# Kernel optimization log

Measured on AMD Instinct MI355X. Metric: run time of the kernel, lower is better.

Reference implementation:

```python
import jax, jax.numpy as jnp
import numpy as np

D_MODEL = 128; NS = 8; D_FF = 512; N_CROSS = 3; N_SELF = 2; PRED = 4
B = 2; N = 5; Q = 2500; HF = 24; WF = 77
VX, VY, VZ = 32, 16, 32  # voxel grid (x, y, z); volume layout [B, C, VY, VX, VZ]


def grid_sample_2d(feat, grid):
    # feat [B,C,H,W]; grid [B,*S,2] xy in [-1,1]; bilinear, align_corners=True, zeros padding
    Bf, C, H, W = feat.shape
    gs = grid.shape[1:-1]
    g = grid.reshape(Bf, -1, 2)
    x = (g[..., 0] + 1.0) * 0.5 * (W - 1)
    y = (g[..., 1] + 1.0) * 0.5 * (H - 1)
    x0 = jnp.floor(x); y0 = jnp.floor(y)
    xd = x - x0; yd = y - y0
    featf = feat.reshape(Bf, C, H * W)
    def corner(xi, yi, w8):
        valid = (xi >= 0) & (xi < W) & (yi >= 0) & (yi < H)
        idx = jnp.clip(yi, 0, H - 1).astype(jnp.int32) * W + jnp.clip(xi, 0, W - 1).astype(jnp.int32)
        gathered = jnp.take_along_axis(featf, idx[:, None, :], axis=2)  # [B,C,P]
        return gathered * (w8 * valid)[:, None, :]
    out = (corner(x0, y0, (1 - xd) * (1 - yd)) + corner(x0 + 1, y0, xd * (1 - yd))
           + corner(x0, y0 + 1, (1 - xd) * yd) + corner(x0 + 1, y0 + 1, xd * yd))
    return out.reshape(Bf, C, *gs)


def grid_sample_3d(feat, grid):
    # feat [B,C,D,H,W]; grid [B,*S,3] with channels (x->W, y->H, z->D); zeros padding
    Bf, C, D, H, W = feat.shape
    gs = grid.shape[1:-1]
    g = grid.reshape(Bf, -1, 3)
    x = (g[..., 0] + 1.0) * 0.5 * (W - 1)
    y = (g[..., 1] + 1.0) * 0.5 * (H - 1)
    z = (g[..., 2] + 1.0) * 0.5 * (D - 1)
    x0 = jnp.floor(x); y0 = jnp.floor(y); z0 = jnp.floor(z)
    xd = x - x0; yd = y - y0; zd = z - z0
    featf = feat.reshape(Bf, C, D * H * W)
    def corner(xi, yi, zi, w8):
        valid = (xi >= 0) & (xi < W) & (yi >= 0) & (yi < H) & (zi >= 0) & (zi < D)
        idx = (jnp.clip(zi, 0, D - 1).astype(jnp.int32) * (H * W)
               + jnp.clip(yi, 0, H - 1).astype(jnp.int32) * W
               + jnp.clip(xi, 0, W - 1).astype(jnp.int32))
        gathered = jnp.take_along_axis(featf, idx[:, None, :], axis=2)
        return gathered * (w8 * valid)[:, None, :]
    out = (corner(x0, y0, z0, (1 - xd) * (1 - yd) * (1 - zd))
           + corner(x0 + 1, y0, z0, xd * (1 - yd) * (1 - zd))
           + corner(x0, y0 + 1, z0, (1 - xd) * yd * (1 - zd))
           + corner(x0 + 1, y0 + 1, z0, xd * yd * (1 - zd))
           + corner(x0, y0, z0 + 1, (1 - xd) * (1 - yd) * zd)
           + corner(x0 + 1, y0, z0 + 1, xd * (1 - yd) * zd)
           + corner(x0, y0 + 1, z0 + 1, (1 - xd) * yd * zd)
           + corner(x0 + 1, y0 + 1, z0 + 1, xd * yd * zd))
    return out.reshape(Bf, C, *gs)


def layer_norm(x, g, b):
    mu = x.mean(-1, keepdims=True)
    var = ((x - mu) ** 2).mean(-1, keepdims=True)
    return (x - mu) / jnp.sqrt(var + 1e-5) * g + b


def setup_inputs() -> dict:
    key = jax.random.key(0)
    ks = iter(jax.random.split(key, 64))
    def rn(shape, scale=0.02):
        return (jax.random.normal(next(ks), shape) * scale).astype(jnp.float32)
    inp = {
        'query': jax.random.normal(next(ks), (B, Q, D_MODEL), jnp.float32),
        'ref_points': jax.random.uniform(next(ks), (B, N, Q, 2), jnp.float32),
        'ref_points_3d': jax.random.uniform(next(ks), (B, Q, 3), jnp.float32) * 2.0 - 1.0,
        'image_features': jax.random.normal(next(ks), (B * N, D_MODEL, HF, WF), jnp.float32),
        'mask': jax.random.randint(next(ks), (B, N, Q), 0, 2) > 0,
        'x_idx': jax.random.randint(next(ks), (B, Q), 0, VX, dtype=jnp.int32),
        'y_idx': jax.random.randint(next(ks), (B, Q), 0, VY, dtype=jnp.int32),
        'z_idx': jax.random.randint(next(ks), (B, Q), 0, VZ, dtype=jnp.int32),
        # cross-attn layers (stacked over N_CROSS)
        'c_ln1_g': jnp.ones((N_CROSS, D_MODEL), jnp.float32), 'c_ln1_b': jnp.zeros((N_CROSS, D_MODEL), jnp.float32),
        'c_dp_w': rn((N_CROSS, D_MODEL, NS * 2)), 'c_dp_b': jnp.zeros((N_CROSS, NS * 2), jnp.float32),
        'c_a_w': rn((N_CROSS, D_MODEL, NS)), 'c_a_b': jnp.zeros((N_CROSS, NS), jnp.float32),
        'c_w_w': rn((N_CROSS, D_MODEL, D_MODEL)), 'c_w_b': jnp.zeros((N_CROSS, D_MODEL), jnp.float32),
        'c_vp_w': rn((N_CROSS, D_MODEL, D_MODEL)), 'c_vp_b': jnp.zeros((N_CROSS, D_MODEL), jnp.float32),
        'c_op_w': rn((N_CROSS, D_MODEL, D_MODEL)), 'c_op_b': jnp.zeros((N_CROSS, D_MODEL), jnp.float32),
        'c_ln2_g': jnp.ones((N_CROSS, D_MODEL), jnp.float32), 'c_ln2_b': jnp.zeros((N_CROSS, D_MODEL), jnp.float32),
        'c_ff1_w': rn((N_CROSS, D_MODEL, D_FF)), 'c_ff1_b': jnp.zeros((N_CROSS, D_FF), jnp.float32),
        'c_ff2_w': rn((N_CROSS, D_FF, D_MODEL)), 'c_ff2_b': jnp.zeros((N_CROSS, D_MODEL), jnp.float32),
        # self-attn layers (stacked over N_SELF)
        's_ln1_g': jnp.ones((N_SELF, D_MODEL), jnp.float32), 's_ln1_b': jnp.zeros((N_SELF, D_MODEL), jnp.float32),
        's_dp_w': rn((N_SELF, D_MODEL, NS * 3)), 's_dp_b': jnp.zeros((N_SELF, NS * 3), jnp.float32),
        's_a_w': rn((N_SELF, D_MODEL, NS)), 's_a_b': jnp.zeros((N_SELF, NS), jnp.float32),
        's_w_w': rn((N_SELF, D_MODEL, D_MODEL)), 's_w_b': jnp.zeros((N_SELF, D_MODEL), jnp.float32),
        's_vp_w': rn((N_SELF, D_MODEL, D_MODEL)), 's_vp_b': jnp.zeros((N_SELF, D_MODEL), jnp.float32),
        's_op_w': rn((N_SELF, D_MODEL, D_MODEL)), 's_op_b': jnp.zeros((N_SELF, D_MODEL), jnp.float32),
        's_ln2_g': jnp.ones((N_SELF, D_MODEL), jnp.float32), 's_ln2_b': jnp.zeros((N_SELF, D_MODEL), jnp.float32),
        's_ff1_w': rn((N_SELF, D_MODEL, D_FF)), 's_ff1_b': jnp.zeros((N_SELF, D_FF), jnp.float32),
        's_ff2_w': rn((N_SELF, D_FF, D_MODEL)), 's_ff2_b': jnp.zeros((N_SELF, D_MODEL), jnp.float32),
        'cls_w': rn((D_MODEL, PRED)), 'cls_b': jnp.zeros((PRED,), jnp.float32),
    }
    return inp


def reference(query, ref_points, ref_points_3d, image_features, mask, x_idx, y_idx, z_idx,
              c_ln1_g, c_ln1_b, c_dp_w, c_dp_b, c_a_w, c_a_b, c_w_w, c_w_b, c_vp_w, c_vp_b,
              c_op_w, c_op_b, c_ln2_g, c_ln2_b, c_ff1_w, c_ff1_b, c_ff2_w, c_ff2_b,
              s_ln1_g, s_ln1_b, s_dp_w, s_dp_b, s_a_w, s_a_b, s_w_w, s_w_b, s_vp_w, s_vp_b,
              s_op_w, s_op_b, s_ln2_g, s_ln2_b, s_ff1_w, s_ff1_b, s_ff2_w, s_ff2_b, cls_w, cls_b):
    mf = mask.astype(query.dtype)  # [B,N,Q]
    flat_idx = y_idx * (VX * VZ) + x_idx * VZ + z_idx  # [B,Q], vol layout [B,C,VY,VX,VZ]
    bb = jnp.arange(B)[:, None]

    # ---- deformable cross attention stack ----
    for i in range(N_CROSS):
        q_ln = layer_norm(query, c_ln1_g[i], c_ln1_b[i])
        dp = (q_ln @ c_dp_w[i] + c_dp_b[i]).reshape(B, Q, NS, 2)
        pd = (ref_points[:, :, :, None, :] + dp[:, None]) * 2.0 - 1.0  # [B,N,Q,Ns,2]
        vf = jnp.einsum('bchw,cd->bdhw', image_features, c_vp_w[i]) + c_vp_b[i][None, :, None, None]
        samp = grid_sample_2d(vf, pd.reshape(B * N, Q, NS, 2))  # [B*N,C,Q,Ns]
        samp = samp.reshape(B, N, D_MODEL, Q, NS).transpose(0, 1, 3, 4, 2)  # [B,N,Q,Ns,C]
        wf = samp @ c_w_w[i] + c_w_b[i]
        att = jax.nn.softmax(q_ln @ c_a_w[i] + c_a_b[i], axis=-1)  # [B,Q,Ns]
        s = (wf * att[:, None, :, :, None]).sum(3)  # [B,N,Q,C]
        s = (s * mf[..., None]).sum(1) / (mf.sum(1)[..., None] + 1e-6)  # masked mean over cameras
        query = query + (s @ c_op_w[i] + c_op_b[i])
        h = layer_norm(query, c_ln2_g[i], c_ln2_b[i])
        h = jax.nn.gelu(h @ c_ff1_w[i] + c_ff1_b[i], approximate=False) @ c_ff2_w[i] + c_ff2_b[i]
        query = query + h

    # ---- voxel scatter + deformable self attention stack ----
    m_any = jnp.any(mask, axis=1).astype(query.dtype)  # [B,Q]
    for i in range(N_SELF):
        vol = jnp.zeros((B, VY * VX * VZ, D_MODEL), query.dtype).at[bb, flat_idx].set(query)
        vol = vol.reshape(B, VY, VX, VZ, D_MODEL).transpose(0, 4, 1, 2, 3)  # [B,C,16,32,32]
        q_ln = layer_norm(query, s_ln1_g[i], s_ln1_b[i])
        dp = (q_ln @ s_dp_w[i] + s_dp_b[i]).reshape(B, Q, NS, 3)
        pd = ref_points_3d[:, :, None, :] + dp
        pd = pd[..., jnp.array([1, 0, 2])]  # permute coords as in torch code
        samp = grid_sample_3d(vol, pd)  # [B,C,Q,Ns]
        samp = samp.transpose(0, 2, 3, 1)  # [B,Q,Ns,C]
        v = samp @ s_vp_w[i] + s_vp_b[i]
        wf = v @ s_w_w[i] + s_w_b[i]
        att = jax.nn.softmax(q_ln @ s_a_w[i] + s_a_b[i], axis=-1)
        s = (wf * att[..., None]).sum(2)  # [B,Q,C]
        s = s * m_any[..., None]
        query = query + (s @ s_op_w[i] + s_op_b[i])
        h = layer_norm(query, s_ln2_g[i], s_ln2_b[i])
        h = jax.nn.gelu(h @ s_ff1_w[i] + s_ff1_b[i], approximate=False) @ s_ff2_w[i] + s_ff2_b[i]
        query = query + h

    logits = query @ cls_w + cls_b  # [B,Q,pred_num]
    return logits
```

## Files before the change

kernel.cpp:

```cpp
#include <hip/hip_runtime.h>
#include <math.h>

#define D_MODELC 128
#define NSAMP 8
#define DFF 512
#define NCROSS 3
#define NSELF 2
#define BB 2
#define NCAM 5
#define QQ 2500
#define HFI 24
#define WFI 77
#define VXC 32
#define VYC 16
#define VZC 32
#define BQ (BB*QQ)
#define HWI (HFI*WFI)
#define NVOX (VYC*VXC*VZC)

typedef float f4 __attribute__((ext_vector_type(4)));
typedef short s8v __attribute__((ext_vector_type(8)));

__device__ __forceinline__ unsigned short f2bf(float f) {
  union { float f; unsigned u; } v; v.f = f;
  unsigned r = v.u + 0x7FFFu + ((v.u >> 16) & 1u);
  return (unsigned short)(r >> 16);
}
__device__ __forceinline__ float bf2f(unsigned short u) {
  union { unsigned u; float f; } v; v.u = ((unsigned)u) << 16; return v.f;
}

__device__ __forceinline__ bool mask_at(const unsigned char* m, int fl, int idx) {
  if (fl) return m[idx] != 0;
  return ((const int*)m)[idx] != 0;
}

__global__ __launch_bounds__(1024) void mask_k(const unsigned char* __restrict__ m,
                                               int* __restrict__ flag,
                                               float* __restrict__ invden, float* __restrict__ imc,
                                               float* __restrict__ many) {
  __shared__ int f;
  if (threadIdx.x == 0) f = 0;
  __syncthreads();
  const int total = BB * NCAM * QQ;
  int loc = 0;
  for (int i = threadIdx.x; i < total; i += 1024)
    if ((i & 3) && m[i]) loc = 1;
  if (loc) atomicOr(&f, 1);
  __syncthreads();
  int fl = f;
  if (threadIdx.x == 0) *flag = fl;
  for (int i = threadIdx.x; i < BQ; i += 1024) {
    int b = i / QQ, q = i % QQ;
    float cnt = 0.f;
    for (int n = 0; n < NCAM; ++n)
      cnt += mask_at(m, fl, (b * NCAM + n) * QQ + q) ? 1.f : 0.f;
    float inv = 1.f / (cnt + 1e-6f);
    invden[i] = inv;
    imc[i] = cnt * inv;
    many[i] = cnt > 0.f ? 1.f : 0.f;
  }
}

__global__ __launch_bounds__(256) void transpose_img_k(const float* __restrict__ in,
                                                       unsigned short* __restrict__ out) {
  __shared__ float til[32][65];
  int bn = blockIdx.z;
  int c0 = blockIdx.y * 32;
  int yx0 = blockIdx.x * 64;
  int t = threadIdx.x;
  {
    int yx_l = t & 63, c_l = t >> 6;
    int yx = yx0 + yx_l;
#pragma unroll
    for (int i = 0; i < 8; ++i) {
      int c = c_l + 4 * i;
      float v = 0.f;
      if (yx < HWI) v = in[((size_t)(bn * D_MODELC + c0 + c)) * HWI + yx];
      til[c][yx_l] = v;
    }
  }
  __syncthreads();
  {
    int yx_l = t >> 2, cc = (t & 3) * 8;
    int yx = yx0 + yx_l;
    if (yx < HWI) {
      union { unsigned short u[8]; s8v v; } pk;
#pragma unroll
      for (int j = 0; j < 8; ++j) pk.u[j] = f2bf(til[cc + j][yx_l]);
      *(s8v*)(out + ((size_t)bn * HWI + yx) * D_MODELC + c0 + cc) = pk.v;
    }
  }
}

__global__ __launch_bounds__(256) void zero_vol_k(unsigned short* __restrict__ vol,
                                                  int* __restrict__ winner) {
  int idx = blockIdx.x * 256 + threadIdx.x;
  const int nv16 = (BB * NVOX * 128) / 8;
  if (idx < nv16) {
    uint4 z = make_uint4(0, 0, 0, 0);
    *(uint4*)(vol + (size_t)idx * 8) = z;
  }
  const int nw4 = (BB * NVOX) / 4;
  if (idx < nw4) {
    int4 m = make_int4(-1, -1, -1, -1);
    *(int4*)(winner + (size_t)idx * 4) = m;
  }
}

__global__ void scatter_winner_k(const int* __restrict__ xi, const int* __restrict__ yi,
                                 const int* __restrict__ zi, int* __restrict__ winner) {
  int i = blockIdx.x * blockDim.x + threadIdx.x;
  if (i >= BQ) return;
  int b = i / QQ;
  int vox = yi[i] * (VXC * VZC) + xi[i] * VZC + zi[i];
  atomicMax(&winner[b * NVOX + vox], i % QQ);
}

__global__ void scatter_write_k(const int* __restrict__ xi, const int* __restrict__ yi,
                                const int* __restrict__ zi, const int* __restrict__ winner,
                                const float* __restrict__ qb, unsigned short* __restrict__ vol) {
  int idx = blockIdx.x * blockDim.x + threadIdx.x;
  if (idx >= BQ * 16) return;
  int g = idx & 15, row = idx >> 4;
  int b = row / QQ, q = row % QQ;
  int vox = yi[row] * (VXC * VZC) + xi[row] * VZC + zi[row];
  if (winner[b * NVOX + vox] != q) return;
  const float* src = qb + (size_t)row * 128 + g * 8;
  float4 a = *(const float4*)src;
  float4 c = *(const float4*)(src + 4);
  union { unsigned short u[8]; s8v v; } pk;
  pk.u[0] = f2bf(a.x); pk.u[1] = f2bf(a.y); pk.u[2] = f2bf(a.z); pk.u[3] = f2bf(a.w);
  pk.u[4] = f2bf(c.x); pk.u[5] = f2bf(c.y); pk.u[6] = f2bf(c.z); pk.u[7] = f2bf(c.w);
  *(s8v*)(vol + ((size_t)b * NVOX + vox) * 128 + g * 8) = pk.v;
}

__global__ __launch_bounds__(256) void tpre_k(const float* __restrict__ c_w_w, const float* __restrict__ s_w_w,
                                              const float* __restrict__ c_op_w, const float* __restrict__ s_op_w,
                                              const float* __restrict__ cf1, const float* __restrict__ sf1,
                                              const float* __restrict__ cf2, const float* __restrict__ sf2,
                                              float* __restrict__ Qbuf,
                                              unsigned short* __restrict__ f1T, unsigned short* __restrict__ f2T) {
  __shared__ float As_[32][64];
  __shared__ float Ws_[32][64];
  int z = blockIdx.z, tid = threadIdx.x;
  if (z < 5) {
    const float* A = (z < 3) ? c_w_w + (size_t)z * 16384 : s_w_w + (size_t)(z - 3) * 16384;
    const float* Bm = (z < 3) ? c_op_w + (size_t)z * 16384 : s_op_w + (size_t)(z - 3) * 16384;
    float* C = Qbuf + (size_t)z * 16384;
    int m0 = blockIdx.x * 64, n0 = blockIdx.y * 64;
    float acc[4][4] = {};
    int mr = (tid >> 4) * 4, nc = (tid & 15) * 4;
    for (int k0 = 0; k0 < 128; k0 += 32) {
      {
        int r = tid >> 2, kq = (tid & 3) * 8;
        const float* ap = A + (size_t)(m0 + r) * 128 + k0 + kq;
        float4 v0 = *(const float4*)ap, v1 = *(const float4*)(ap + 4);
        As_[kq + 0][r] = v0.x; As_[kq + 1][r] = v0.y; As_[kq + 2][r] = v0.z; As_[kq + 3][r] = v0.w;
        As_[kq + 4][r] = v1.x; As_[kq + 5][r] = v1.y; As_[kq + 6][r] = v1.z; As_[kq + 7][r] = v1.w;
      }
      {
        int kr = tid >> 3, nq = (tid & 7) * 8;
        const float* wp = Bm + (size_t)(k0 + kr) * 128 + n0 + nq;
        *(float4*)&Ws_[kr][nq] = *(const float4*)wp;
        *(float4*)&Ws_[kr][nq + 4] = *(const float4*)(wp + 4);
      }
      __syncthreads();
#pragma unroll
      for (int kk = 0; kk < 32; ++kk) {
        float4 av = *(const float4*)&As_[kk][mr];
        float4 bv = *(const float4*)&Ws_[kk][nc];
        float a_[4] = {av.x, av.y, av.z, av.w};
        float b_[4] = {bv.x, bv.y, bv.z, bv.w};
#pragma unroll
        for (int i = 0; i < 4; ++i)
#pragma unroll
          for (int j = 0; j < 4; ++j) acc[i][j] += a_[i] * b_[j];
      }
      __syncthreads();
    }
#pragma unroll
    for (int i = 0; i < 4; ++i) {
      float4 r;
      r.x = acc[i][0]; r.y = acc[i][1]; r.z = acc[i][2]; r.w = acc[i][3];
      *(float4*)(C + (size_t)(m0 + mr + i) * 128 + n0 + nc) = r;
    }
  } else {
    int bid = (z - 5) * 4 + blockIdx.y * 2 + blockIdx.x;
    int widx = bid >> 6, chunk = bid & 63;
    const float* src; unsigned short* dst; int K, N;
    if (widx < 5) {
      src = (widx < 3) ? cf1 + (size_t)widx * 65536 : sf1 + (size_t)(widx - 3) * 65536;
      dst = f1T + (size_t)widx * 65536; K = 128; N = 512;
    } else {
      int L = widx - 5;
      src = (L < 3) ? cf2 + (size_t)L * 65536 : sf2 + (size_t)(L - 3) * 65536;
      dst = f2T + (size_t)L * 65536; K = 512; N = 128;
    }
    int e = (chunk * 256 + tid) * 4;
    int k = e % K, n = e / K;
    ushort4 o;
    o.x = f2bf(src[(size_t)(k + 0) * N + n]);
    o.y = f2bf(src[(size_t)(k + 1) * N + n]);
    o.z = f2bf(src[(size_t)(k + 2) * N + n]);
    o.w = f2bf(src[(size_t)(k + 3) * N + n]);
    *(ushort4*)(dst + e) = o;
  }
}

struct P5 { const float* a[5]; const float* b[5]; float* c[5]; };

__global__ __launch_bounds__(256) void small_mm_k(P5 ps) {
  const float* A = ps.a[blockIdx.z];
  const float* Bm = ps.b[blockIdx.z];
  float* C = ps.c[blockIdx.z];
  __shared__ float As_[32][64];
  __shared__ float Ws_[32][64];
  int m0 = blockIdx.x * 64, n0 = blockIdx.y * 64, tid = threadIdx.x;
  float acc[4][4] = {};
  int mr = (tid >> 4) * 4, nc = (tid & 15) * 4;
  for (int k0 = 0; k0 < 128; k0 += 32) {
    {
      int r = tid >> 2, kq = (tid & 3) * 8;
      const float* ap = A + (size_t)(m0 + r) * 128 + k0 + kq;
      float4 v0 = *(const float4*)ap, v1 = *(const float4*)(ap + 4);
      As_[kq + 0][r] = v0.x; As_[kq + 1][r] = v0.y; As_[kq + 2][r] = v0.z; As_[kq + 3][r] = v0.w;
      As_[kq + 4][r] = v1.x; As_[kq + 5][r] = v1.y; As_[kq + 6][r] = v1.z; As_[kq + 7][r] = v1.w;
    }
    {
      int kr = tid >> 3, nq = (tid & 7) * 8;
      const float* wp = Bm + (size_t)(k0 + kr) * 128 + n0 + nq;
      *(float4*)&Ws_[kr][nq] = *(const float4*)wp;
      *(float4*)&Ws_[kr][nq + 4] = *(const float4*)(wp + 4);
    }
    __syncthreads();
#pragma unroll
    for (int kk = 0; kk < 32; ++kk) {
      float4 av = *(const float4*)&As_[kk][mr];
      float4 bv = *(const float4*)&Ws_[kk][nc];
      float a_[4] = {av.x, av.y, av.z, av.w};
      float b_[4] = {bv.x, bv.y, bv.z, bv.w};
#pragma unroll
      for (int i = 0; i < 4; ++i)
#pragma unroll
        for (int j = 0; j < 4; ++j) acc[i][j] += a_[i] * b_[j];
    }
    __syncthreads();
  }
#pragma unroll
  for (int i = 0; i < 4; ++i) {
    float4 r;
    r.x = acc[i][0]; r.y = acc[i][1]; r.z = acc[i][2]; r.w = acc[i][3];
    *(float4*)(C + (size_t)(m0 + mr + i) * 128 + n0 + nc) = r;
  }
}

__global__ __launch_bounds__(256) void wpre_k(const float* __restrict__ Wcbuf,
                                              unsigned short* __restrict__ WcT,
                                              const float* __restrict__ c_vp_b, const float* __restrict__ c_w_b,
                                              const float* __restrict__ s_vp_b, const float* __restrict__ s_w_b,
                                              const float* __restrict__ c_op_w, const float* __restrict__ s_op_w,
                                              const float* __restrict__ Qbuf,
                                              float* __restrict__ v1buf, float* __restrict__ v2buf,
                                              float* __restrict__ csbuf) {
  int t = threadIdx.x;
  if (blockIdx.y < 5) {
    int L = blockIdx.y;
    const float* src = Wcbuf + (size_t)L * 16384;
    unsigned short* dst = WcT + (size_t)L * 16384;
    int e = (blockIdx.x * 256 + t) * 4;
    int k = e & 127, n = e >> 7;
    ushort4 o;
    o.x = f2bf(src[(size_t)(k + 0) * 128 + n]);
    o.y = f2bf(src[(size_t)(k + 1) * 128 + n]);
    o.z = f2bf(src[(size_t)(k + 2) * 128 + n]);
    o.w = f2bf(src[(size_t)(k + 3) * 128 + n]);
    *(ushort4*)(dst + e) = o;
  } else if (blockIdx.x < 5 && t < 128) {
    int L = blockIdx.x, n = t;
    const float* vpb = L < 3 ? c_vp_b + L * 128 : s_vp_b + (L - 3) * 128;
    const float* wb = L < 3 ? c_w_b + L * 128 : s_w_b + (L - 3) * 128;
    const float* op = L < 3 ? c_op_w + (size_t)L * 16384 : s_op_w + (size_t)(L - 3) * 16384;
    const float* Q = Qbuf + (size_t)L * 16384;
    float a = 0.f, c = 0.f;
    for (int k = 0; k < 128; ++k) {
      a += vpb[k] * Q[k * 128 + n];
      c += wb[k] * op[k * 128 + n];
    }
    if (L < 3) { v1buf[L * 128 + n] = a; v2buf[L * 128 + n] = c; }
    else csbuf[(L - 3) * 128 + n] = a + c;
  }
}

__global__ __launch_bounds__(512) void cross_mega_k(
    const float* __restrict__ query, const float* __restrict__ refp,
    const unsigned char* __restrict__ maskp, const int* __restrict__ flagp,
    const float* __restrict__ invden, const float* __restrict__ imc,
    const unsigned short* __restrict__ imgT,
    const float* __restrict__ ln1g, const float* __restrict__ ln1b,
    const float* __restrict__ dpw_, const float* __restrict__ dpb_,
    const float* __restrict__ aw_, const float* __restrict__ ab_,
    const unsigned short* __restrict__ WcT, const float* __restrict__ opb_,
    const float* __restrict__ v1_, const float* __restrict__ v2_,
    const float* __restrict__ ln2g, const float* __restrict__ ln2b,
    const unsigned short* __restrict__ f1T, const float* __restrict__ b1_,
    const unsigned short* __restrict__ f2T, const float* __restrict__ b2_,
    float* __restrict__ qb, int M) {
  __shared__ float qtile[16][128];
  __shared__ float pr[16][32];
  __shared__ float attL[16][8];
  __shared__ float awa[16];
  __shared__ __align__(16) unsigned short As[16 * 128];
  __shared__ __align__(16) char scratch[20480];
  int* soff = (int*)scratch;
  float* sw = (float*)(scratch + 10240);
  float* wl = (float*)scratch;
  unsigned short* Hs = (unsigned short*)scratch;

  int t = threadIdx.x;
  int m0 = blockIdx.x * 16;
  int r5 = t >> 5, cg5 = t & 31;
  int row5 = m0 + r5;
  int w = t >> 6, l = t & 63, la = l & 15, lb = l >> 4;
  int fl = *flagp;
  {
    float4 v = make_float4(0, 0, 0, 0);
    if (row5 < M) v = *(const float4*)(query + (size_t)row5 * 128 + cg5 * 4);
    *(float4*)&qtile[r5][cg5 * 4] = v;
  }
  __syncthreads();

  for (int L = 0; L < NCROSS; ++L) {
    const float* dpw = dpw_ + (size_t)L * 2048;
    const float* dpb = dpb_ + L * 16;
    const float* aw = aw_ + (size_t)L * 1024;
    const float* ab = ab_ + L * 8;
    const float* g1 = ln1g + L * 128;
    const float* be1 = ln1b + L * 128;
    for (int idx = t; idx < 24 * 128; idx += 512) {
      int c = idx >> 7, k = idx & 127;
      wl[c * 132 + k] = (c < 16) ? dpw[k * 16 + c] : aw[k * 8 + (c - 16)];
    }
    __syncthreads();
    {
      float4 v = *(const float4*)&qtile[r5][cg5 * 4];
      float s1 = v.x + v.y + v.z + v.w;
      float s2 = v.x * v.x + v.y * v.y + v.z * v.z + v.w * v.w;
#pragma unroll
      for (int msk = 1; msk < 32; msk <<= 1) { s1 += __shfl_xor(s1, msk); s2 += __shfl_xor(s2, msk); }
      float mean = s1 * (1.f / 128.f);
      float var = s2 * (1.f / 128.f) - mean * mean;
      float inv = rsqrtf(var + 1e-5f);
      float lv[4] = {v.x, v.y, v.z, v.w};
      float ln4[4];
#pragma unroll
      for (int i = 0; i < 4; ++i) {
        int k = cg5 * 4 + i;
        ln4[i] = (lv[i] - mean) * inv * g1[k] + be1[k];
      }
      float p[24];
#pragma unroll
      for (int c = 0; c < 24; ++c) {
        float acc = 0.f;
#pragma unroll
        for (int i = 0; i < 4; ++i) acc += ln4[i] * wl[c * 132 + cg5 * 4 + i];
        p[c] = acc;
      }
#pragma unroll
      for (int msk = 1; msk < 32; msk <<= 1) {
#pragma unroll
        for (int c = 0; c < 24; ++c) p[c] += __shfl_xor(p[c], msk);
      }
      if (cg5 == 0) {
#pragma unroll
        for (int c = 0; c < 24; ++c) pr[r5][c] = p[c];
      }
    }
    __syncthreads();
    {
      int cc = cg5 & 7;
      float av = pr[r5][16 + cc] + ab[cc];
      float mx = av;
#pragma unroll
      for (int msk = 1; msk < 8; msk <<= 1) mx = fmaxf(mx, __shfl_xor(mx, msk));
      float e = expf(av - mx);
      float sm = e;
#pragma unroll
      for (int msk = 1; msk < 8; msk <<= 1) sm += __shfl_xor(sm, msk);
      if (cg5 < 8) attL[r5][cg5] = e / sm;
    }
    __syncthreads();
    for (int e = t; e < 640; e += 512) {
      int qi = e / 40, rem = e % 40;
      int n = rem >> 3, s = rem & 7;
      int row = m0 + qi;
      if (row >= M) {
#pragma unroll
        for (int c = 0; c < 4; ++c) { soff[e * 4 + c] = 0; sw[e * 4 + c] = 0.f; }
      } else {
        int b = row / QQ, q = row - b * QQ;
        int mi = (b * NCAM + n) * QQ + q;
        bool mk = mask_at(maskp, fl, mi);
        float a = mk ? attL[qi][s] : 0.f;
        float rx = refp[(size_t)mi * 2 + 0];
        float ry = refp[(size_t)mi * 2 + 1];
        float fx = (rx + pr[qi][s * 2 + 0] + dpb[s * 2 + 0]) * (float)(WFI - 1);
        float fy = (ry + pr[qi][s * 2 + 1] + dpb[s * 2 + 1]) * (float)(HFI - 1);
        float x0f = floorf(fx), y0f = floorf(fy);
        int x0 = (int)x0f, y0 = (int)y0f;
        float xd = fx - x0f, yd = fy - y0f;
        int base = (b * NCAM + n) * HWI;
#pragma unroll
        for (int cy = 0; cy < 2; ++cy)
#pragma unroll
          for (int cx = 0; cx < 2; ++cx) {
            int xi = x0 + cx, yi = y0 + cy;
            bool ok = (xi >= 0) & (xi < WFI) & (yi >= 0) & (yi < HFI);
            int xc = min(max(xi, 0), WFI - 1), yc = min(max(yi, 0), HFI - 1);
            soff[e * 4 + cy * 2 + cx] = (base + yc * WFI + xc) * 128;
            sw[e * 4 + cy * 2 + cx] = ok ? a * (cx ? xd : 1.f - xd) * (cy ? yd : 1.f - yd) : 0.f;
          }
      }
    }
    __syncthreads();
    {
      int qi = t >> 5, sub = t & 31, ln = sub & 15, half = sub >> 4;
      float acc[8] = {};
      float wa = 0.f;
      for (int e = half * 20; e < half * 20 + 20; ++e) {
        int eb = qi * 40 + e;
        float4 wv = *(const float4*)&sw[eb * 4];
        float wsum = wv.x + wv.y + wv.z + wv.w;
        if (wsum != 0.f) {
          int4 ov = *(const int4*)&soff[eb * 4];
          s8v p0 = *(const s8v*)(imgT + (size_t)ov.x + ln * 8);
          s8v p1 = *(const s8v*)(imgT + (size_t)ov.y + ln * 8);
          s8v p2 = *(const s8v*)(imgT + (size_t)ov.z + ln * 8);
          s8v p3 = *(const s8v*)(imgT + (size_t)ov.w + ln * 8);
#pragma unroll
          for (int i = 0; i < 8; ++i)
            acc[i] += wv.x * bf2f((unsigned short)p0[i]) + wv.y * bf2f((unsigned short)p1[i])
                    + wv.z * bf2f((unsigned short)p2[i]) + wv.w * bf2f((unsigned short)p3[i]);
          wa += wsum;
        }
      }
#pragma unroll
      for (int i = 0; i < 8; ++i) acc[i] += __shfl_xor(acc[i], 16);
      wa += __shfl_xor(wa, 16);
      if (half == 0) {
        union { unsigned short u[8]; s8v v; } pk;
#pragma unroll
        for (int i = 0; i < 8; ++i) pk.u[i] = f2bf(acc[i]);
        *(s8v*)&As[qi * 128 + ((ln ^ (qi & 7)) << 3)] = pk.v;
        if (ln == 0) awa[qi] = wa;
      }
    }
    __syncthreads();
    {
      const unsigned short* Wc = WcT + (size_t)L * 16384;
      const float* v1L = v1_ + L * 128;
      const float* v2L = v2_ + L * 128;
      const float* opbL = opb_ + L * 128;
      f4 accm = {};
      int col = w * 16 + la;
#pragma unroll
      for (int ks = 0; ks < 4; ++ks) {
        s8v af = *(const s8v*)&As[la * 128 + (((ks * 4 + lb) ^ (la & 7)) << 3)];
        s8v bf = *(const s8v*)(Wc + (size_t)col * 128 + ks * 32 + lb * 8);
        accm = __builtin_amdgcn_mfma_f32_16x16x32_bf16(af, bf, accm, 0, 0, 0);
      }
#pragma unroll
      for (int j = 0; j < 4; ++j) {
        int lr = lb * 4 + j;
        int m = m0 + lr;
        if (m < M) {
          float s0m = invden[m];
          float val = accm[j] * s0m + s0m * awa[lr] * v1L[col] + imc[m] * v2L[col] + opbL[col];
          qtile[lr][col] += val;
        }
      }
    }
    __syncthreads();
    {
      const float* g2 = ln2g + L * 128;
      const float* be2 = ln2b + L * 128;
      float4 v = *(const float4*)&qtile[r5][cg5 * 4];
      float s1 = v.x + v.y + v.z + v.w;
      float s2 = v.x * v.x + v.y * v.y + v.z * v.z + v.w * v.w;
#pragma unroll
      for (int msk = 1; msk < 32; msk <<= 1) { s1 += __shfl_xor(s1, msk); s2 += __shfl_xor(s2, msk); }
      float mean = s1 * (1.f / 128.f);
      float var = s2 * (1.f / 128.f) - mean * mean;
      float inv = rsqrtf(var + 1e-5f);
      float lv[4] = {v.x, v.y, v.z, v.w};
      union { unsigned short u[4]; ushort4 v4; } pk;
#pragma unroll
      for (int i = 0; i < 4; ++i) {
        int k = cg5 * 4 + i;
        pk.u[i] = f2bf((lv[i] - mean) * inv * g2[k] + be2[k]);
      }
      int c8 = cg5 >> 1, hf = cg5 & 1;
      *(ushort4*)&As[r5 * 128 + ((c8 ^ (r5 & 7)) << 3) + hf * 4] = pk.v4;
    }
    __syncthreads();
    {
      const unsigned short* W1 = f1T + (size_t)L * 65536;
      const float* b1 = b1_ + L * 512;
      f4 acc1[4] = {};
#pragma unroll
      for (int ks = 0; ks < 4; ++ks) {
        s8v af = *(const s8v*)&As[la * 128 + (((ks * 4 + lb) ^ (la & 7)) << 3)];
#pragma unroll
        for (int ti = 0; ti < 4; ++ti) {
          int col = (w * 4 + ti) * 16 + la;
          s8v bf = *(const s8v*)(W1 + (size_t)col * 128 + ks * 32 + lb * 8);
          acc1[ti] = __builtin_amdgcn_mfma_f32_16x16x32_bf16(af, bf, acc1[ti], 0, 0, 0);
        }
      }
#pragma unroll
      for (int ti = 0; ti < 4; ++ti) {
        int col = (w * 4 + ti) * 16 + la;
        int chunk = col >> 3, idx = col & 7;
#pragma unroll
        for (int j = 0; j < 4; ++j) {
          int m = lb * 4 + j;
          float val = acc1[ti][j] + b1[col];
          val = 0.5f * val * (1.f + erff(val * 0.70710678118654752f));
          Hs[m * 512 + ((chunk ^ (m & 7)) << 3) + idx] = f2bf(val);
        }
      }
    }
    __syncthreads();
    {
      const unsigned short* W2 = f2T + (size_t)L * 65536;
      const float* b2 = b2_ + L * 128;
      f4 acc2 = {};
      int col = w * 16 + la;
#pragma unroll
      for (int ks = 0; ks < 16; ++ks) {
        s8v af = *(const s8v*)&Hs[la * 512 + (((ks * 4 + lb) ^ (la & 7)) << 3)];
        s8v bf = *(const s8v*)(W2 + (size_t)col * 512 + ks * 32 + lb * 8);
        acc2 = __builtin_amdgcn_mfma_f32_16x16x32_bf16(af, bf, acc2, 0, 0, 0);
      }
#pragma unroll
      for (int j = 0; j < 4; ++j) qtile[lb * 4 + j][col] += acc2[j] + b2[col];
    }
    __syncthreads();
  }
  if (row5 < M)
    *(float4*)(qb + (size_t)row5 * 128 + cg5 * 4) = *(const float4*)&qtile[r5][cg5 * 4];
}

template <bool CLS>
__global__ __launch_bounds__(512) void self_mega_k(
    const float* __restrict__ qbin, const float* __restrict__ ref3d,
    const unsigned short* __restrict__ vol, const float* __restrict__ many,
    const float* __restrict__ ln1g, const float* __restrict__ ln1b,
    const float* __restrict__ dpw, const float* __restrict__ dpb,
    const float* __restrict__ aw, const float* __restrict__ ab,
    const unsigned short* __restrict__ WcT, const float* __restrict__ opb,
    const float* __restrict__ csb,
    const float* __restrict__ ln2g, const float* __restrict__ ln2b,
    const unsigned short* __restrict__ f1T, const float* __restrict__ b1,
    const unsigned short* __restrict__ f2T, const float* __restrict__ b2,
    float* __restrict__ qb,
    const float* __restrict__ cw, const float* __restrict__ cb, float* __restrict__ out,
    int M) {
  __shared__ float qtile[16][128];
  __shared__ float pr[16][32];
  __shared__ float attL[16][8];
  __shared__ float gcL[16][24];
  __shared__ __align__(16) unsigned short As[16 * 128];
  __shared__ __align__(16) char scratch[20480];
  int* soff = (int*)scratch;
  float* sw = (float*)(scratch + 4096);
  float* wl = (float*)scratch;
  unsigned short* Hs = (unsigned short*)scratch;

  int t = threadIdx.x;
  int m0 = blockIdx.x * 16;
  int r5 = t >> 5, cg5 = t & 31;
  int row5 = m0 + r5;
  int w = t >> 6, l = t & 63, la = l & 15, lb = l >> 4;
  {
    float4 v = make_float4(0, 0, 0, 0);
    if (row5 < M) v = *(const float4*)(qbin + (size_t)row5 * 128 + cg5 * 4);
    *(float4*)&qtile[r5][cg5 * 4] = v;
  }
  for (int idx = t; idx < 32 * 128; idx += 512) {
    int c = idx >> 7, k = idx & 127;
    wl[c * 132 + k] = (c < 24) ? dpw[k * 24 + c] : aw[k * 8 + (c - 24)];
  }
  __syncthreads();
  {
    float4 v = *(const float4*)&qtile[r5][cg5 * 4];
    float s1 = v.x + v.y + v.z + v.w;
    float s2 = v.x * v.x + v.y * v.y + v.z * v.z + v.w * v.w;
#pragma unroll
    for (int msk = 1; msk < 32; msk <<= 1) { s1 += __shfl_xor(s1, msk); s2 += __shfl_xor(s2, msk); }
    float mean = s1 * (1.f / 128.f);
    float var = s2 * (1.f / 128.f) - mean * mean;
    float inv = rsqrtf(var + 1e-5f);
    float lv[4] = {v.x, v.y, v.z, v.w};
    float ln4[4];
#pragma unroll
    for (int i = 0; i < 4; ++i) {
      int k = cg5 * 4 + i;
      ln4[i] = (lv[i] - mean) * inv * ln1g[k] + ln1b[k];
    }
    float p[32];
#pragma unroll
    for (int c = 0; c < 32; ++c) {
      float acc = 0.f;
#pragma unroll
      for (int i = 0; i < 4; ++i) acc += ln4[i] * wl[c * 132 + cg5 * 4 + i];
      p[c] = acc;
    }
#pragma unroll
    for (int msk = 1; msk < 32; msk <<= 1) {
#pragma unroll
      for (int c = 0; c < 32; ++c) p[c] += __shfl_xor(p[c], msk);
    }
    if (cg5 == 0) {
#pragma unroll
      for (int c = 0; c < 32; ++c) pr[r5][c] = p[c];
    }
  }
  __syncthreads();
  {
    int cc = cg5 & 7;
    float av = pr[r5][24 + cc] + ab[cc];
    float mx = av;
#pragma unroll
    for (int msk = 1; msk < 8; msk <<= 1) mx = fmaxf(mx, __shfl_xor(mx, msk));
    float e = expf(av - mx);
    float sm = e;
#pragma unroll
    for (int msk = 1; msk < 8; msk <<= 1) sm += __shfl_xor(sm, msk);
    if (cg5 < 8) attL[r5][cg5] = e / sm;
  }
  if (t < 384) {
    int r = t / 24, tt = t % 24;
    int s = tt / 3, j = tt % 3;
    int pc = (j == 0) ? 1 : ((j == 1) ? 0 : 2);
    int row = m0 + r;
    float rv = (row < M) ? ref3d[row * 3 + pc] : 0.f;
    gcL[r][tt] = pr[r][s * 3 + pc] + dpb[s * 3 + pc] + rv;
  }
  __syncthreads();
  if (t < 128) {
    int qi = t >> 3, s = t & 7;
    int row = m0 + qi;
    if (row >= M) {
#pragma unroll
      for (int c = 0; c < 8; ++c) { soff[t * 8 + c] = 0; sw[t * 8 + c] = 0.f; }
    } else {
      int b = row / QQ;
      float a = attL[qi][s];
      float fx = (gcL[qi][s * 3 + 0] + 1.f) * 0.5f * (float)(VZC - 1);
      float fy = (gcL[qi][s * 3 + 1] + 1.f) * 0.5f * (float)(VXC - 1);
      float fz = (gcL[qi][s * 3 + 2] + 1.f) * 0.5f * (float)(VYC - 1);
      float x0f = floorf(fx), y0f = floorf(fy), z0f = floorf(fz);
      int x0 = (int)x0f, y0 = (int)y0f, z0 = (int)z0f;
      float xd = fx - x0f, yd = fy - y0f, zd = fz - z0f;
      int base = b * NVOX;
#pragma unroll
      for (int cz = 0; cz < 2; ++cz)
#pragma unroll
        for (int cy = 0; cy < 2; ++cy)
#pragma unroll
          for (int cx = 0; cx < 2; ++cx) {
            int xi = x0 + cx, yi = y0 + cy, zi = z0 + cz;
            bool ok = (xi >= 0) & (xi < VZC) & (yi >= 0) & (yi < VXC) & (zi >= 0) & (zi < VYC);
            int xc = min(max(xi, 0), VZC - 1);
            int yc = min(max(yi, 0), VXC - 1);
            int zc = min(max(zi, 0), VYC - 1);
            int ci = cz * 4 + cy * 2 + cx;
            soff[t * 8 + ci] = (base + (zc * VXC + yc) * VZC + xc) * 128;
            sw[t * 8 + ci] = ok ? a * (cx ? xd : 1.f - xd) * (cy ? yd : 1.f - yd) * (cz ? zd : 1.f - zd) : 0.f;
          }
    }
  }
  __syncthreads();
  {
    int qi = t >> 5, sub = t & 31, ln = sub & 15, half = sub >> 4;
    float acc[8] = {};
    for (int s = half * 4; s < half * 4 + 4; ++s) {
      int eb = qi * 8 + s;
#pragma unroll
      for (int c = 0; c < 8; ++c) {
        float wgt = sw[eb * 8 + c];
        if (wgt != 0.f) {
          s8v p = *(const s8v*)(vol + (size_t)soff[eb * 8 + c] + ln * 8);
#pragma unroll
          for (int i = 0; i < 8; ++i) acc[i] += wgt * bf2f((unsigned short)p[i]);
        }
      }
    }
#pragma unroll
    for (int i = 0; i < 8; ++i) acc[i] += __shfl_xor(acc[i], 16);
    if (half == 0) {
      union { unsigned short u[8]; s8v v; } pk;
#pragma unroll
      for (int i = 0; i < 8; ++i) pk.u[i] = f2bf(acc[i]);
      *(s8v*)&As[qi * 128 + ((ln ^ (qi & 7)) << 3)] = pk.v;
    }
  }
  __syncthreads();
  {
    f4 accm = {};
    int col = w * 16 + la;
#pragma unroll
    for (int ks = 0; ks < 4; ++ks) {
      s8v af = *(const s8v*)&As[la * 128 + (((ks * 4 + lb) ^ (la & 7)) << 3)];
      s8v bf = *(const s8v*)(WcT + (size_t)col * 128 + ks * 32 + lb * 8);
      accm = __builtin_amdgcn_mfma_f32_16x16x32_bf16(af, bf, accm, 0, 0, 0);
    }
#pragma unroll
    for (int j = 0; j < 4; ++j) {
      int lr = lb * 4 + j;
      int m = m0 + lr;
      if (m < M) {
        float s0m = many[m];
        qtile[lr][col] += accm[j] * s0m + s0m * csb[col] + opb[col];
      }
    }
  }
  __syncthreads();
  {
    float4 v = *(const float4*)&qtile[r5][cg5 * 4];
    float s1 = v.x + v.y + v.z + v.w;
    float s2 = v.x * v.x + v.y * v.y + v.z * v.z + v.w * v.w;
#pragma unroll
    for (int msk = 1; msk < 32; msk <<= 1) { s1 += __shfl_xor(s1, msk); s2 += __shfl_xor(s2, msk); }
    float mean = s1 * (1.f / 128.f);
    float var = s2 * (1.f / 128.f) - mean * mean;
    float inv = rsqrtf(var + 1e-5f);
    float lv[4] = {v.x, v.y, v.z, v.w};
    union { unsigned short u[4]; ushort4 v4; } pk;
#pragma unroll
    for (int i = 0; i < 4; ++i) {
      int k = cg5 * 4 + i;
      pk.u[i] = f2bf((lv[i] - mean) * inv * ln2g[k] + ln2b[k]);
    }
    int c8 = cg5 >> 1, hf = cg5 & 1;
    *(ushort4*)&As[r5 * 128 + ((c8 ^ (r5 & 7)) << 3) + hf * 4] = pk.v4;
  }
  __syncthreads();
  {
    f4 acc1[4] = {};
#pragma unroll
    for (int ks = 0; ks < 4; ++ks) {
      s8v af = *(const s8v*)&As[la * 128 + (((ks * 4 + lb) ^ (la & 7)) << 3)];
#pragma unroll
      for (int ti = 0; ti < 4; ++ti) {
        int col = (w * 4 + ti) * 16 + la;
        s8v bf = *(const s8v*)(f1T + (size_t)col * 128 + ks * 32 + lb * 8);
        acc1[ti] = __builtin_amdgcn_mfma_f32_16x16x32_bf16(af, bf, acc1[ti], 0, 0, 0);
      }
    }
#pragma unroll
    for (int ti = 0; ti < 4; ++ti) {
      int col = (w * 4 + ti) * 16 + la;
      int chunk = col >> 3, idx = col & 7;
#pragma unroll
      for (int j = 0; j < 4; ++j) {
        int m = lb * 4 + j;
        float val = acc1[ti][j] + b1[col];
        val = 0.5f * val * (1.f + erff(val * 0.70710678118654752f));
        Hs[m * 512 + ((chunk ^ (m & 7)) << 3) + idx] = f2bf(val);
      }
    }
  }
  __syncthreads();
  {
    f4 acc2 = {};
    int col = w * 16 + la;
#pragma unroll
    for (int ks = 0; ks < 16; ++ks) {
      s8v af = *(const s8v*)&Hs[la * 512 + (((ks * 4 + lb) ^ (la & 7)) << 3)];
      s8v bf = *(const s8v*)(f2T + (size_t)col * 512 + ks * 32 + lb * 8);
      acc2 = __builtin_amdgcn_mfma_f32_16x16x32_bf16(af, bf, acc2, 0, 0, 0);
    }
#pragma unroll
    for (int j = 0; j < 4; ++j) qtile[lb * 4 + j][col] += acc2[j] + b2[col];
  }
  __syncthreads();
  if (CLS) {
    float ps0 = 0.f, ps1 = 0.f, ps2 = 0.f, ps3 = 0.f;
#pragma unroll
    for (int i = 0; i < 4; ++i) {
      int k = cg5 * 4 + i;
      float qv = qtile[r5][k];
      ps0 += qv * cw[k * 4 + 0];
      ps1 += qv * cw[k * 4 + 1];
      ps2 += qv * cw[k * 4 + 2];
      ps3 += qv * cw[k * 4 + 3];
    }
#pragma unroll
    for (int msk = 1; msk < 32; msk <<= 1) {
      ps0 += __shfl_xor(ps0, msk);
      ps1 += __shfl_xor(ps1, msk);
      ps2 += __shfl_xor(ps2, msk);
      ps3 += __shfl_xor(ps3, msk);
    }
    if (cg5 < 4 && row5 < M) {
      float o = (cg5 == 0) ? ps0 : (cg5 == 1) ? ps1 : (cg5 == 2) ? ps2 : ps3;
      out[row5 * 4 + cg5] = o + cb[cg5];
    }
  } else {
    if (row5 < M)
      *(float4*)(qb + (size_t)row5 * 128 + cg5 * 4) = *(const float4*)&qtile[r5][cg5 * 4];
  }
}

extern "C" void kernel_launch(void* const* d_in, const int* in_sizes, int n_in,
                              void* d_out, int out_size, void* d_ws, size_t ws_size,
                              hipStream_t stream) {
  (void)in_sizes; (void)n_in; (void)out_size; (void)ws_size;
  const float* query = (const float*)d_in[0];
  const float* ref_points = (const float*)d_in[1];
  const float* ref3d = (const float*)d_in[2];
  const float* imgf = (const float*)d_in[3];
  const unsigned char* maskp = (const unsigned char*)d_in[4];
  const int* x_idx = (const int*)d_in[5];
  const int* y_idx = (const int*)d_in[6];
  const int* z_idx = (const int*)d_in[7];
  const float* c_ln1_g = (const float*)d_in[8];
  const float* c_ln1_b = (const float*)d_in[9];
  const float* c_dp_w = (const float*)d_in[10];
  const float* c_dp_b = (const float*)d_in[11];
  const float* c_a_w = (const float*)d_in[12];
  const float* c_a_b = (const float*)d_in[13];
  const float* c_w_w = (const float*)d_in[14];
  const float* c_w_b = (const float*)d_in[15];
  const float* c_vp_w = (const float*)d_in[16];
  const float* c_vp_b = (const float*)d_in[17];
  const float* c_op_w = (const float*)d_in[18];
  const float* c_op_b = (const float*)d_in[19];
  const float* c_ln2_g = (const float*)d_in[20];
  const float* c_ln2_b = (const float*)d_in[21];
  const float* c_ff1_w = (const float*)d_in[22];
  const float* c_ff1_b = (const float*)d_in[23];
  const float* c_ff2_w = (const float*)d_in[24];
  const float* c_ff2_b = (const float*)d_in[25];
  const float* s_ln1_g = (const float*)d_in[26];
  const float* s_ln1_b = (const float*)d_in[27];
  const float* s_dp_w = (const float*)d_in[28];
  const float* s_dp_b = (const float*)d_in[29];
  const float* s_a_w = (const float*)d_in[30];
  const float* s_a_b = (const float*)d_in[31];
  const float* s_w_w = (const float*)d_in[32];
  const float* s_w_b = (const float*)d_in[33];
  const float* s_vp_w = (const float*)d_in[34];
  const float* s_vp_b = (const float*)d_in[35];
  const float* s_op_w = (const float*)d_in[36];
  const float* s_op_b = (const float*)d_in[37];
  const float* s_ln2_g = (const float*)d_in[38];
  const float* s_ln2_b = (const float*)d_in[39];
  const float* s_ff1_w = (const float*)d_in[40];
  const float* s_ff1_b = (const float*)d_in[41];
  const float* s_ff2_w = (const float*)d_in[42];
  const float* s_ff2_b = (const float*)d_in[43];
  const float* cls_w = (const float*)d_in[44];
  const float* cls_b = (const float*)d_in[45];
  float* out = (float*)d_out;

  char* ws = (char*)d_ws;
  size_t off = 0;
  auto carve = [&](size_t bytes) -> char* {
    char* p = ws + off;
    off += (bytes + 255) & ~(size_t)255;
    return p;
  };
  int* flag = (int*)carve(256);
  float* invden = (float*)carve(BQ * 4);
  float* imc = (float*)carve(BQ * 4);
  float* many = (float*)carve(BQ * 4);
  float* qb = (float*)carve((size_t)BQ * 128 * 4);
  int* winner = (int*)carve((size_t)BB * NVOX * 4);
  float* Qbuf = (float*)carve((size_t)5 * 16384 * 4);
  float* Wcbuf = (float*)carve((size_t)5 * 16384 * 4);
  unsigned short* WcT = (unsigned short*)carve((size_t)5 * 16384 * 2);
  unsigned short* f1T = (unsigned short*)carve((size_t)5 * 65536 * 2);
  unsigned short* f2T = (unsigned short*)carve((size_t)5 * 65536 * 2);
  float* v1buf = (float*)carve(3 * 128 * 4);
  float* v2buf = (float*)carve(3 * 128 * 4);
  float* csbuf = (float*)carve(2 * 128 * 4);
  unsigned short* imgT = (unsigned short*)carve((size_t)BB * NCAM * HWI * 128 * 2);
  unsigned short* vol = (unsigned short*)carve((size_t)BB * NVOX * 128 * 2);

  const int M = BQ;
  const int GB16 = (M + 15) / 16;

  mask_k<<<1, 1024, 0, stream>>>(maskp, flag, invden, imc, many);
  tpre_k<<<dim3(2, 2, 165), 256, 0, stream>>>(c_w_w, s_w_w, c_op_w, s_op_w,
                                              c_ff1_w, s_ff1_w, c_ff2_w, s_ff2_w,
                                              Qbuf, f1T, f2T);
  {
    P5 pw;
    for (int L = 0; L < 5; ++L) {
      pw.a[L] = (L < 3) ? c_vp_w + (size_t)L * 16384 : s_vp_w + (size_t)(L - 3) * 16384;
      pw.b[L] = Qbuf + (size_t)L * 16384;
      pw.c[L] = Wcbuf + (size_t)L * 16384;
    }
    small_mm_k<<<dim3(2, 2, 5), 256, 0, stream>>>(pw);
  }
  wpre_k<<<dim3(16, 6), 256, 0, stream>>>(Wcbuf, WcT, c_vp_b, c_w_b, s_vp_b, s_w_b,
                                          c_op_w, s_op_w, Qbuf, v1buf, v2buf, csbuf);
  transpose_img_k<<<dim3((HWI + 63) / 64, 4, BB * NCAM), 256, 0, stream>>>(imgf, imgT);
  zero_vol_k<<<1024, 256, 0, stream>>>(vol, winner);
  scatter_winner_k<<<(BQ + 255) / 256, 256, 0, stream>>>(x_idx, y_idx, z_idx, winner);

  cross_mega_k<<<GB16, 512, 0, stream>>>(query, ref_points, maskp, flag, invden, imc, imgT,
                                         c_ln1_g, c_ln1_b, c_dp_w, c_dp_b, c_a_w, c_a_b,
                                         WcT, c_op_b, v1buf, v2buf, c_ln2_g, c_ln2_b,
                                         f1T, c_ff1_b, f2T, c_ff2_b, qb, M);

  scatter_write_k<<<(BQ * 16 + 255) / 256, 256, 0, stream>>>(x_idx, y_idx, z_idx, winner, qb, vol);
  self_mega_k<false><<<GB16, 512, 0, stream>>>(qb, ref3d, vol, many,
                                               s_ln1_g, s_ln1_b, s_dp_w, s_dp_b, s_a_w, s_a_b,
                                               WcT + (size_t)3 * 16384, s_op_b, csbuf,
                                               s_ln2_g, s_ln2_b,
                                               f1T + (size_t)3 * 65536, s_ff1_b,
                                               f2T + (size_t)3 * 65536, s_ff2_b,
                                               qb, cls_w, cls_b, out, M);
  scatter_write_k<<<(BQ * 16 + 255) / 256, 256, 0, stream>>>(x_idx, y_idx, z_idx, winner, qb, vol);
  self_mega_k<true><<<GB16, 512, 0, stream>>>(qb, ref3d, vol, many,
                                              s_ln1_g + 128, s_ln1_b + 128,
                                              s_dp_w + (size_t)128 * 24, s_dp_b + 24,
                                              s_a_w + (size_t)128 * 8, s_a_b + 8,
                                              WcT + (size_t)4 * 16384, s_op_b + 128,
                                              csbuf + 128, s_ln2_g + 128, s_ln2_b + 128,
                                              f1T + (size_t)4 * 65536, s_ff1_b + 512,
                                              f2T + (size_t)4 * 65536, s_ff2_b + 128,
                                              qb, cls_w, cls_b, out, M);
}
```

Before: 471.5 us.

## Halve rows per block in cross/self mega kernels to double grid size

The fused cross- and self-attention kernels now handle 8 query rows per 512-thread block instead of 16, so the grid doubles to 625 blocks and more CUs are busy. Each wave owns one row for layer norm and projections, and softmax is computed per sampling thread, which removes a barrier. MFMA tiles stay 16 rows wide, so the upper 8 rows are zero-padded and half of the matrix work is wasted. Bounds checks on M are dropped because BQ divides evenly by 8, and the zero-weight skip in the gather loop is removed.

```diff
diff --git a/kernel.cpp b/kernel.cpp
--- a/kernel.cpp
+++ b/kernel.cpp
@@ -305,28 +305,27 @@
     const float* __restrict__ ln2g, const float* __restrict__ ln2b,
     const unsigned short* __restrict__ f1T, const float* __restrict__ b1_,
     const unsigned short* __restrict__ f2T, const float* __restrict__ b2_,
-    float* __restrict__ qb, int M) {
-  __shared__ float qtile[16][128];
-  __shared__ float pr[16][32];
-  __shared__ float attL[16][8];
-  __shared__ float awa[16];
+    float* __restrict__ qb) {
+  __shared__ float qtile[8][136];
+  __shared__ float pr[8][24];
+  __shared__ float awa[8];
   __shared__ __align__(16) unsigned short As[16 * 128];
-  __shared__ __align__(16) char scratch[20480];
+  __shared__ __align__(16) char scratch[16896];
   int* soff = (int*)scratch;
-  float* sw = (float*)(scratch + 10240);
+  float* sw = (float*)(scratch + 5120);
   float* wl = (float*)scratch;
   unsigned short* Hs = (unsigned short*)scratch;
 
   int t = threadIdx.x;
-  int m0 = blockIdx.x * 16;
-  int r5 = t >> 5, cg5 = t & 31;
-  int row5 = m0 + r5;
-  int w = t >> 6, l = t & 63, la = l & 15, lb = l >> 4;
+  int m0 = blockIdx.x * 8;
+  int wv = t >> 6, lane = t & 63;
+  int la = lane & 15, lb = lane >> 4;
   int fl = *flagp;
-  {
-    float4 v = make_float4(0, 0, 0, 0);
-    if (row5 < M) v = *(const float4*)(query + (size_t)row5 * 128 + cg5 * 4);
-    *(float4*)&qtile[r5][cg5 * 4] = v;
+  if (lane < 32)
+    *(float4*)&qtile[wv][lane * 4] = *(const float4*)(query + (size_t)(m0 + wv) * 128 + lane * 4);
+  if (t < 128) {
+    s8v z = {};
+    *(s8v*)&As[(8 + (t >> 4)) * 128 + (t & 15) * 8] = z;
   }
   __syncthreads();
 
@@ -343,111 +342,92 @@
     }
     __syncthreads();
     {
-      float4 v = *(const float4*)&qtile[r5][cg5 * 4];
-      float s1 = v.x + v.y + v.z + v.w;
-      float s2 = v.x * v.x + v.y * v.y + v.z * v.z + v.w * v.w;
-#pragma unroll
-      for (int msk = 1; msk < 32; msk <<= 1) { s1 += __shfl_xor(s1, msk); s2 += __shfl_xor(s2, msk); }
+      int c0 = lane * 2;
+      float x0 = qtile[wv][c0], x1 = qtile[wv][c0 + 1];
+      float s1 = x0 + x1, s2 = x0 * x0 + x1 * x1;
+#pragma unroll
+      for (int msk = 1; msk < 64; msk <<= 1) { s1 += __shfl_xor(s1, msk); s2 += __shfl_xor(s2, msk); }
       float mean = s1 * (1.f / 128.f);
       float var = s2 * (1.f / 128.f) - mean * mean;
       float inv = rsqrtf(var + 1e-5f);
-      float lv[4] = {v.x, v.y, v.z, v.w};
-      float ln4[4];
-#pragma unroll
-      for (int i = 0; i < 4; ++i) {
-        int k = cg5 * 4 + i;
-        ln4[i] = (lv[i] - mean) * inv * g1[k] + be1[k];
-      }
+      float l0 = (x0 - mean) * inv * g1[c0] + be1[c0];
+      float l1 = (x1 - mean) * inv * g1[c0 + 1] + be1[c0 + 1];
       float p[24];
 #pragma unroll
-      for (int c = 0; c < 24; ++c) {
-        float acc = 0.f;
-#pragma unroll
-        for (int i = 0; i < 4; ++i) acc += ln4[i] * wl[c * 132 + cg5 * 4 + i];
-        p[c] = acc;
-      }
-#pragma unroll
-      for (int msk = 1; msk < 32; msk <<= 1) {
+      for (int c = 0; c < 24; ++c)
+        p[c] = l0 * wl[c * 132 + c0] + l1 * wl[c * 132 + c0 + 1];
+#pragma unroll
+      for (int msk = 1; msk < 64; msk <<= 1) {
 #pragma unroll
         for (int c = 0; c < 24; ++c) p[c] += __shfl_xor(p[c], msk);
       }
-      if (cg5 == 0) {
-#pragma unroll
-        for (int c = 0; c < 24; ++c) pr[r5][c] = p[c];
-      }
-    }
-    __syncthreads();
-    {
-      int cc = cg5 & 7;
-      float av = pr[r5][16 + cc] + ab[cc];
-      float mx = av;
-#pragma unroll
-      for (int msk = 1; msk < 8; msk <<= 1) mx = fmaxf(mx, __shfl_xor(mx, msk));
-      float e = expf(av - mx);
-      float sm = e;
-#pragma unroll
-      for (int msk = 1; msk < 8; msk <<= 1) sm += __shfl_xor(sm, msk);
-      if (cg5 < 8) attL[r5][cg5] = e / sm;
-    }
-    __syncthreads();
-    for (int e = t; e < 640; e += 512) {
-      int qi = e / 40, rem = e % 40;
+      if (lane == 0) {
+#pragma unroll
+        for (int c = 0; c < 24; ++c) pr[wv][c] = p[c];
+      }
+    }
+    __syncthreads();
+    if (t < 320) {
+      int qi = t / 40, rem = t % 40;
       int n = rem >> 3, s = rem & 7;
       int row = m0 + qi;
-      if (row >= M) {
-#pragma unroll
-        for (int c = 0; c < 4; ++c) { soff[e * 4 + c] = 0; sw[e * 4 + c] = 0.f; }
-      } else {
-        int b = row / QQ, q = row - b * QQ;
-        int mi = (b * NCAM + n) * QQ + q;
-        bool mk = mask_at(maskp, fl, mi);
-        float a = mk ? attL[qi][s] : 0.f;
-        float rx = refp[(size_t)mi * 2 + 0];
-        float ry = refp[(size_t)mi * 2 + 1];
-        float fx = (rx + pr[qi][s * 2 + 0] + dpb[s * 2 + 0]) * (float)(WFI - 1);
-        float fy = (ry + pr[qi][s * 2 + 1] + dpb[s * 2 + 1]) * (float)(HFI - 1);
-        float x0f = floorf(fx), y0f = floorf(fy);
-        int x0 = (int)x0f, y0 = (int)y0f;
-        float xd = fx - x0f, yd = fy - y0f;
-        int base = (b * NCAM + n) * HWI;
-#pragma unroll
-        for (int cy = 0; cy < 2; ++cy)
-#pragma unroll
-          for (int cx = 0; cx < 2; ++cx) {
-            int xi = x0 + cx, yi = y0 + cy;
-            bool ok = (xi >= 0) & (xi < WFI) & (yi >= 0) & (yi < HFI);
-            int xc = min(max(xi, 0), WFI - 1), yc = min(max(yi, 0), HFI - 1);
-            soff[e * 4 + cy * 2 + cx] = (base + yc * WFI + xc) * 128;
-            sw[e * 4 + cy * 2 + cx] = ok ? a * (cx ? xd : 1.f - xd) * (cy ? yd : 1.f - yd) : 0.f;
-          }
-      }
+      int b = row / QQ, q = row - b * QQ;
+      int mi = (b * NCAM + n) * QQ + q;
+      bool mk = mask_at(maskp, fl, mi);
+      float mx = -1e30f;
+      float av[8];
+#pragma unroll
+      for (int i = 0; i < 8; ++i) { av[i] = pr[qi][16 + i] + ab[i]; mx = fmaxf(mx, av[i]); }
+      float sm = 0.f, es = 0.f;
+#pragma unroll
+      for (int i = 0; i < 8; ++i) {
+        float e_ = expf(av[i] - mx);
+        sm += e_;
+        if (i == s) es = e_;
+      }
+      float a = mk ? es / sm : 0.f;
+      float rx = refp[(size_t)mi * 2 + 0];
+      float ry = refp[(size_t)mi * 2 + 1];
+      float fx = (rx + pr[qi][s * 2 + 0] + dpb[s * 2 + 0]) * (float)(WFI - 1);
+      float fy = (ry + pr[qi][s * 2 + 1] + dpb[s * 2 + 1]) * (float)(HFI - 1);
+      float x0f = floorf(fx), y0f = floorf(fy);
+      int x0 = (int)x0f, y0 = (int)y0f;
+      float xd = fx - x0f, yd = fy - y0f;
+      int base = (b * NCAM + n) * HWI;
+#pragma unroll
+      for (int cy = 0; cy < 2; ++cy)
+#pragma unroll
+        for (int cx = 0; cx < 2; ++cx) {
+          int xi = x0 + cx, yi = y0 + cy;
+          bool ok = (xi >= 0) & (xi < WFI) & (yi >= 0) & (yi < HFI);
+          int xc = min(max(xi, 0), WFI - 1), yc = min(max(yi, 0), HFI - 1);
+          soff[t * 4 + cy * 2 + cx] = (base + yc * WFI + xc) * 128;
+          sw[t * 4 + cy * 2 + cx] = ok ? a * (cx ? xd : 1.f - xd) * (cy ? yd : 1.f - yd) : 0.f;
+        }
     }
     __syncthreads();
     {
-      int qi = t >> 5, sub = t & 31, ln = sub & 15, half = sub >> 4;
+      int qi = wv, ln = lane & 15, eg = lane >> 4;
       float acc[8] = {};
       float wa = 0.f;
-      for (int e = half * 20; e < half * 20 + 20; ++e) {
+      for (int e = eg * 10; e < eg * 10 + 10; ++e) {
         int eb = qi * 40 + e;
-        float4 wv = *(const float4*)&sw[eb * 4];
-        float wsum = wv.x + wv.y + wv.z + wv.w;
-        if (wsum != 0.f) {
-          int4 ov = *(const int4*)&soff[eb * 4];
-          s8v p0 = *(const s8v*)(imgT + (size_t)ov.x + ln * 8);
-          s8v p1 = *(const s8v*)(imgT + (size_t)ov.y + ln * 8);
-          s8v p2 = *(const s8v*)(imgT + (size_t)ov.z + ln * 8);
-          s8v p3 = *(const s8v*)(imgT + (size_t)ov.w + ln * 8);
-#pragma unroll
-          for (int i = 0; i < 8; ++i)
-            acc[i] += wv.x * bf2f((unsigned short)p0[i]) + wv.y * bf2f((unsigned short)p1[i])
-                    + wv.z * bf2f((unsigned short)p2[i]) + wv.w * bf2f((unsigned short)p3[i]);
-          wa += wsum;
-        }
-      }
-#pragma unroll
-      for (int i = 0; i < 8; ++i) acc[i] += __shfl_xor(acc[i], 16);
-      wa += __shfl_xor(wa, 16);
-      if (half == 0) {
+        float4 wv4 = *(const float4*)&sw[eb * 4];
+        int4 ov = *(const int4*)&soff[eb * 4];
+        s8v p0 = *(const s8v*)(imgT + (size_t)ov.x + ln * 8);
+        s8v p1 = *(const s8v*)(imgT + (size_t)ov.y + ln * 8);
+        s8v p2 = *(const s8v*)(imgT + (size_t)ov.z + ln * 8);
+        s8v p3 = *(const s8v*)(imgT + (size_t)ov.w + ln * 8);
+#pragma unroll
+        for (int i = 0; i < 8; ++i)
+          acc[i] += wv4.x * bf2f((unsigned short)p0[i]) + wv4.y * bf2f((unsigned short)p1[i])
+                  + wv4.z * bf2f((unsigned short)p2[i]) + wv4.w * bf2f((unsigned short)p3[i]);
+        wa += wv4.x + wv4.y + wv4.z + wv4.w;
+      }
+#pragma unroll
+      for (int i = 0; i < 8; ++i) { acc[i] += __shfl_xor(acc[i], 16); acc[i] += __shfl_xor(acc[i], 32); }
+      wa += __shfl_xor(wa, 16); wa += __shfl_xor(wa, 32);
+      if (eg == 0) {
         union { unsigned short u[8]; s8v v; } pk;
 #pragma unroll
         for (int i = 0; i < 8; ++i) pk.u[i] = f2bf(acc[i]);
@@ -462,7 +442,7 @@
       const float* v2L = v2_ + L * 128;
       const float* opbL = opb_ + L * 128;
       f4 accm = {};
-      int col = w * 16 + la;
+      int col = wv * 16 + la;
 #pragma unroll
       for (int ks = 0; ks < 4; ++ks) {
         s8v af = *(const s8v*)&As[la * 128 + (((ks * 4 + lb) ^ (la & 7)) << 3)];
@@ -472,11 +452,10 @@
 #pragma unroll
       for (int j = 0; j < 4; ++j) {
         int lr = lb * 4 + j;
-        int m = m0 + lr;
-        if (m < M) {
+        if (lr < 8) {
+          int m = m0 + lr;
           float s0m = invden[m];
-          float val = accm[j] * s0m + s0m * awa[lr] * v1L[col] + imc[m] * v2L[col] + opbL[col];
-          qtile[lr][col] += val;
+          qtile[lr][col] += accm[j] * s0m + s0m * awa[lr] * v1L[col] + imc[m] * v2L[col] + opbL[col];
         }
       }
     }
@@ -484,23 +463,18 @@
     {
       const float* g2 = ln2g + L * 128;
       const float* be2 = ln2b + L * 128;
-      float4 v = *(const float4*)&qtile[r5][cg5 * 4];
-      float s1 = v.x + v.y + v.z + v.w;
-      float s2 = v.x * v.x + v.y * v.y + v.z * v.z + v.w * v.w;
-#pragma unroll
-      for (int msk = 1; msk < 32; msk <<= 1) { s1 += __shfl_xor(s1, msk); s2 += __shfl_xor(s2, msk); }
+      int c0 = lane * 2;
+      float x0 = qtile[wv][c0], x1 = qtile[wv][c0 + 1];
+      float s1 = x0 + x1, s2 = x0 * x0 + x1 * x1;
+#pragma unroll
+      for (int msk = 1; msk < 64; msk <<= 1) { s1 += __shfl_xor(s1, msk); s2 += __shfl_xor(s2, msk); }
       float mean = s1 * (1.f / 128.f);
       float var = s2 * (1.f / 128.f) - mean * mean;
       float inv = rsqrtf(var + 1e-5f);
-      float lv[4] = {v.x, v.y, v.z, v.w};
-      union { unsigned short u[4]; ushort4 v4; } pk;
-#pragma unroll
-      for (int i = 0; i < 4; ++i) {
-        int k = cg5 * 4 + i;
-        pk.u[i] = f2bf((lv[i] - mean) * inv * g2[k] + be2[k]);
-      }
-      int c8 = cg5 >> 1, hf = cg5 & 1;
-      *(ushort4*)&As[r5 * 128 + ((c8 ^ (r5 & 7)) << 3) + hf * 4] = pk.v4;
+      unsigned u0 = f2bf((x0 - mean) * inv * g2[c0] + be2[c0]);
+      unsigned u1 = f2bf((x1 - mean) * inv * g2[c0 + 1] + be2[c0 + 1]);
+      int chunk = lane >> 2, idx2 = (lane & 3) * 2;
+      *(unsigned*)&As[wv * 128 + ((chunk ^ (wv & 7)) << 3) + idx2] = u0 | (u1 << 16);
     }
     __syncthreads();
     {
@@ -512,20 +486,23 @@
         s8v af = *(const s8v*)&As[la * 128 + (((ks * 4 + lb) ^ (la & 7)) << 3)];
 #pragma unroll
         for (int ti = 0; ti < 4; ++ti) {
-          int col = (w * 4 + ti) * 16 + la;
+          int col = (wv * 4 + ti) * 16 + la;
           s8v bf = *(const s8v*)(W1 + (size_t)col * 128 + ks * 32 + lb * 8);
           acc1[ti] = __builtin_amdgcn_mfma_f32_16x16x32_bf16(af, bf, acc1[ti], 0, 0, 0);
         }
       }
 #pragma unroll
       for (int ti = 0; ti < 4; ++ti) {
-        int col = (w * 4 + ti) * 16 + la;
+        int col = (wv * 4 + ti) * 16 + la;
         int chunk = col >> 3, idx = col & 7;
 #pragma unroll
         for (int j = 0; j < 4; ++j) {
           int m = lb * 4 + j;
-          float val = acc1[ti][j] + b1[col];
-          val = 0.5f * val * (1.f + erff(val * 0.70710678118654752f));
+          float val = 0.f;
+          if (m < 8) {
+            val = acc1[ti][j] + b1[col];
+            val = 0.5f * val * (1.f + erff(val * 0.70710678118654752f));
+          }
           Hs[m * 512 + ((chunk ^ (m & 7)) << 3) + idx] = f2bf(val);
         }
       }
@@ -535,7 +512,7 @@
       const unsigned short* W2 = f2T + (size_t)L * 65536;
       const float* b2 = b2_ + L * 128;
       f4 acc2 = {};
-      int col = w * 16 + la;
+      int col = wv * 16 + la;
 #pragma unroll
       for (int ks = 0; ks < 16; ++ks) {
         s8v af = *(const s8v*)&Hs[la * 512 + (((ks * 4 + lb) ^ (la & 7)) << 3)];
@@ -543,12 +520,15 @@
         acc2 = __builtin_amdgcn_mfma_f32_16x16x32_bf16(af, bf, acc2, 0, 0, 0);
       }
 #pragma unroll
-      for (int j = 0; j < 4; ++j) qtile[lb * 4 + j][col] += acc2[j] + b2[col];
-    }
-    __syncthreads();
-  }
-  if (row5 < M)
-    *(float4*)(qb + (size_t)row5 * 128 + cg5 * 4) = *(const float4*)&qtile[r5][cg5 * 4];
+      for (int j = 0; j < 4; ++j) {
+        int lr = lb * 4 + j;
+        if (lr < 8) qtile[lr][col] += acc2[j] + b2[col];
+      }
+    }
+    __syncthreads();
+  }
+  if (lane < 32)
+    *(float4*)(qb + (size_t)(m0 + wv) * 128 + lane * 4) = *(const float4*)&qtile[wv][lane * 4];
 }
 
 template <bool CLS>
@@ -564,28 +544,25 @@
     const unsigned short* __restrict__ f1T, const float* __restrict__ b1,
     const unsigned short* __restrict__ f2T, const float* __restrict__ b2,
     float* __restrict__ qb,
-    const float* __restrict__ cw, const float* __restrict__ cb, float* __restrict__ out,
-    int M) {
-  __shared__ float qtile[16][128];
-  __shared__ float pr[16][32];
-  __shared__ float attL[16][8];
-  __shared__ float gcL[16][24];
+    const float* __restrict__ cw, const float* __restrict__ cb, float* __restrict__ out) {
+  __shared__ float qtile[8][136];
+  __shared__ float pr[8][32];
   __shared__ __align__(16) unsigned short As[16 * 128];
-  __shared__ __align__(16) char scratch[20480];
+  __shared__ __align__(16) char scratch[16896];
   int* soff = (int*)scratch;
-  float* sw = (float*)(scratch + 4096);
+  float* sw = (float*)(scratch + 2048);
   float* wl = (float*)scratch;
   unsigned short* Hs = (unsigned short*)scratch;
 
   int t = threadIdx.x;
-  int m0 = blockIdx.x * 16;
-  int r5 = t >> 5, cg5 = t & 31;
-  int row5 = m0 + r5;
-  int w = t >> 6, l = t & 63, la = l & 15, lb = l >> 4;
-  {
-    float4 v = make_float4(0, 0, 0, 0);
-    if (row5 < M) v = *(const float4*)(qbin + (size_t)row5 * 128 + cg5 * 4);
-    *(float4*)&qtile[r5][cg5 * 4] = v;
+  int m0 = blockIdx.x * 8;
+  int wv = t >> 6, lane = t & 63;
+  int la = lane & 15, lb = lane >> 4;
+  if (lane < 32)
+    *(float4*)&qtile[wv][lane * 4] = *(const float4*)(qbin + (size_t)(m0 + wv) * 128 + lane * 4);
+  if (t < 128) {
+    s8v z = {};
+    *(s8v*)&As[(8 + (t >> 4)) * 128 + (t & 15) * 8] = z;
   }
   for (int idx = t; idx < 32 * 128; idx += 512) {
     int c = idx >> 7, k = idx & 127;
@@ -593,113 +570,91 @@
   }
   __syncthreads();
   {
-    float4 v = *(const float4*)&qtile[r5][cg5 * 4];
-    float s1 = v.x + v.y + v.z + v.w;
-    float s2 = v.x * v.x + v.y * v.y + v.z * v.z + v.w * v.w;
-#pragma unroll
-    for (int msk = 1; msk < 32; msk <<= 1) { s1 += __shfl_xor(s1, msk); s2 += __shfl_xor(s2, msk); }
+    int c0 = lane * 2;
+    float x0 = qtile[wv][c0], x1 = qtile[wv][c0 + 1];
+    float s1 = x0 + x1, s2 = x0 * x0 + x1 * x1;
+#pragma unroll
+    for (int msk = 1; msk < 64; msk <<= 1) { s1 += __shfl_xor(s1, msk); s2 += __shfl_xor(s2, msk); }
     float mean = s1 * (1.f / 128.f);
     float var = s2 * (1.f / 128.f) - mean * mean;
     float inv = rsqrtf(var + 1e-5f);
-    float lv[4] = {v.x, v.y, v.z, v.w};
-    float ln4[4];
-#pragma unroll
-    for (int i = 0; i < 4; ++i) {
-      int k = cg5 * 4 + i;
-      ln4[i] = (lv[i] - mean) * inv * ln1g[k] + ln1b[k];
-    }
+    float l0 = (x0 - mean) * inv * ln1g[c0] + ln1b[c0];
+    float l1 = (x1 - mean) * inv * ln1g[c0 + 1] + ln1b[c0 + 1];
     float p[32];
 #pragma unroll
-    for (int c = 0; c < 32; ++c) {
-      float acc = 0.f;
-#pragma unroll
-      for (int i = 0; i < 4; ++i) acc += ln4[i] * wl[c * 132 + cg5 * 4 + i];
-      p[c] = acc;
-    }
-#pragma unroll
-    for (int msk = 1; msk < 32; msk <<= 1) {
+    for (int c = 0; c < 32; ++c)
+      p[c] = l0 * wl[c * 132 + c0] + l1 * wl[c * 132 + c0 + 1];
+#pragma unroll
+    for (int msk = 1; msk < 64; msk <<= 1) {
 #pragma unroll
       for (int c = 0; c < 32; ++c) p[c] += __shfl_xor(p[c], msk);
     }
-    if (cg5 == 0) {
-#pragma unroll
-      for (int c = 0; c < 32; ++c) pr[r5][c] = p[c];
-    }
-  }
-  __syncthreads();
-  {
-    int cc = cg5 & 7;
-    float av = pr[r5][24 + cc] + ab[cc];
-    float mx = av;
-#pragma unroll
-    for (int msk = 1; msk < 8; msk <<= 1) mx = fmaxf(mx, __shfl_xor(mx, msk));
-    float e = expf(av - mx);
-    float sm = e;
-#pragma unroll
-    for (int msk = 1; msk < 8; msk <<= 1) sm += __shfl_xor(sm, msk);
-    if (cg5 < 8) attL[r5][cg5] = e / sm;
-  }
-  if (t < 384) {
-    int r = t / 24, tt = t % 24;
-    int s = tt / 3, j = tt % 3;
-    int pc = (j == 0) ? 1 : ((j == 1) ? 0 : 2);
-    int row = m0 + r;
-    float rv = (row < M) ? ref3d[row * 3 + pc] : 0.f;
-    gcL[r][tt] = pr[r][s * 3 + pc] + dpb[s * 3 + pc] + rv;
-  }
-  __syncthreads();
-  if (t < 128) {
+    if (lane == 0) {
+#pragma unroll
+      for (int c = 0; c < 32; ++c) pr[wv][c] = p[c];
+    }
+  }
+  __syncthreads();
+  if (t < 64) {
     int qi = t >> 3, s = t & 7;
     int row = m0 + qi;
-    if (row >= M) {
-#pragma unroll
-      for (int c = 0; c < 8; ++c) { soff[t * 8 + c] = 0; sw[t * 8 + c] = 0.f; }
-    } else {
-      int b = row / QQ;
-      float a = attL[qi][s];
-      float fx = (gcL[qi][s * 3 + 0] + 1.f) * 0.5f * (float)(VZC - 1);
-      float fy = (gcL[qi][s * 3 + 1] + 1.f) * 0.5f * (float)(VXC - 1);
-      float fz = (gcL[qi][s * 3 + 2] + 1.f) * 0.5f * (float)(VYC - 1);
-      float x0f = floorf(fx), y0f = floorf(fy), z0f = floorf(fz);
-      int x0 = (int)x0f, y0 = (int)y0f, z0 = (int)z0f;
-      float xd = fx - x0f, yd = fy - y0f, zd = fz - z0f;
-      int base = b * NVOX;
-#pragma unroll
-      for (int cz = 0; cz < 2; ++cz)
-#pragma unroll
-        for (int cy = 0; cy < 2; ++cy)
-#pragma unroll
-          for (int cx = 0; cx < 2; ++cx) {
-            int xi = x0 + cx, yi = y0 + cy, zi = z0 + cz;
-            bool ok = (xi >= 0) & (xi < VZC) & (yi >= 0) & (yi < VXC) & (zi >= 0) & (zi < VYC);
-            int xc = min(max(xi, 0), VZC - 1);
-            int yc = min(max(yi, 0), VXC - 1);
-            int zc = min(max(zi, 0), VYC - 1);
-            int ci = cz * 4 + cy * 2 + cx;
-            soff[t * 8 + ci] = (base + (zc * VXC + yc) * VZC + xc) * 128;
-            sw[t * 8 + ci] = ok ? a * (cx ? xd : 1.f - xd) * (cy ? yd : 1.f - yd) * (cz ? zd : 1.f - zd) : 0.f;
-          }
-    }
+    int b = row / QQ;
+    float mx = -1e30f;
+    float av[8];
+#pragma unroll
+    for (int i = 0; i < 8; ++i) { av[i] = pr[qi][24 + i] + ab[i]; mx = fmaxf(mx, av[i]); }
+    float sm = 0.f, es = 0.f;
+#pragma unroll
+    for (int i = 0; i < 8; ++i) {
+      float e_ = expf(av[i] - mx);
+      sm += e_;
+      if (i == s) es = e_;
+    }
+    float a = es / sm;
+    float g0 = pr[qi][s * 3 + 1] + dpb[s * 3 + 1] + ref3d[row * 3 + 1];
+    float g1v = pr[qi][s * 3 + 0] + dpb[s * 3 + 0] + ref3d[row * 3 + 0];
+    float g2v = pr[qi][s * 3 + 2] + dpb[s * 3 + 2] + ref3d[row * 3 + 2];
+    float fx = (g0 + 1.f) * 0.5f * (float)(VZC - 1);
+    float fy = (g1v + 1.f) * 0.5f * (float)(VXC - 1);
+    float fz = (g2v + 1.f) * 0.5f * (float)(VYC - 1);
+    float x0f = floorf(fx), y0f = floorf(fy), z0f = floorf(fz);
+    int x0 = (int)x0f, y0 = (int)y0f, z0 = (int)z0f;
+    float xd = fx - x0f, yd = fy - y0f, zd = fz - z0f;
+    int base = b * NVOX;
+#pragma unroll
+    for (int cz = 0; cz < 2; ++cz)
+#pragma unroll
+      for (int cy = 0; cy < 2; ++cy)
+#pragma unroll
+        for (int cx = 0; cx < 2; ++cx) {
+          int xi = x0 + cx, yi = y0 + cy, zi = z0 + cz;
+          bool ok = (xi >= 0) & (xi < VZC) & (yi >= 0) & (yi < VXC) & (zi >= 0) & (zi < VYC);
+          int xc = min(max(xi, 0), VZC - 1);
+          int yc = min(max(yi, 0), VXC - 1);
+          int zc = min(max(zi, 0), VYC - 1);
+          int ci = cz * 4 + cy * 2 + cx;
+          soff[t * 8 + ci] = (base + (zc * VXC + yc) * VZC + xc) * 128;
+          sw[t * 8 + ci] = ok ? a * (cx ? xd : 1.f - xd) * (cy ? yd : 1.f - yd) * (cz ? zd : 1.f - zd) : 0.f;
+        }
   }
   __syncthreads();
   {
-    int qi = t >> 5, sub = t & 31, ln = sub & 15, half = sub >> 4;
+    int qi = wv, ln = lane & 15, eg = lane >> 4;
     float acc[8] = {};
-    for (int s = half * 4; s < half * 4 + 4; ++s) {
-      int eb = qi * 8 + s;
+#pragma unroll
+    for (int ss = 0; ss < 2; ++ss) {
+      int eb = qi * 8 + eg * 2 + ss;
 #pragma unroll
       for (int c = 0; c < 8; ++c) {
         float wgt = sw[eb * 8 + c];
-        if (wgt != 0.f) {
-          s8v p = *(const s8v*)(vol + (size_t)soff[eb * 8 + c] + ln * 8);
-#pragma unroll
-          for (int i = 0; i < 8; ++i) acc[i] += wgt * bf2f((unsigned short)p[i]);
-        }
-      }
-    }
-#pragma unroll
-    for (int i = 0; i < 8; ++i) acc[i] += __shfl_xor(acc[i], 16);
-    if (half == 0) {
+        s8v p = *(const s8v*)(vol + (size_t)soff[eb * 8 + c] + ln * 8);
+#pragma unroll
+        for (int i = 0; i < 8; ++i) acc[i] += wgt * bf2f((unsigned short)p[i]);
+      }
+    }
+#pragma unroll
+    for (int i = 0; i < 8; ++i) { acc[i] += __shfl_xor(acc[i], 16); acc[i] += __shfl_xor(acc[i], 32); }
+    if (eg == 0) {
       union { unsigned short u[8]; s8v v; } pk;
 #pragma unroll
       for (int i = 0; i < 8; ++i) pk.u[i] = f2bf(acc[i]);
@@ -709,7 +664,7 @@
   __syncthreads();
   {
     f4 accm = {};
-    int col = w * 16 + la;
+    int col = wv * 16 + la;
 #pragma unroll
     for (int ks = 0; ks < 4; ++ks) {
       s8v af = *(const s8v*)&As[la * 128 + (((ks * 4 + lb) ^ (la & 7)) << 3)];
@@ -719,8 +674,8 @@
 #pragma unroll
     for (int j = 0; j < 4; ++j) {
       int lr = lb * 4 + j;
-      int m = m0 + lr;
-      if (m < M) {
+      if (lr < 8) {
+        int m = m0 + lr;
         float s0m = many[m];
         qtile[lr][col] += accm[j] * s0m + s0m * csb[col] + opb[col];
       }
@@ -728,23 +683,18 @@
   }
   __syncthreads();
   {
-    float4 v = *(const float4*)&qtile[r5][cg5 * 4];
-    float s1 = v.x + v.y + v.z + v.w;
-    float s2 = v.x * v.x + v.y * v.y + v.z * v.z + v.w * v.w;
-#pragma unroll
-    for (int msk = 1; msk < 32; msk <<= 1) { s1 += __shfl_xor(s1, msk); s2 += __shfl_xor(s2, msk); }
+    int c0 = lane * 2;
+    float x0 = qtile[wv][c0], x1 = qtile[wv][c0 + 1];
+    float s1 = x0 + x1, s2 = x0 * x0 + x1 * x1;
+#pragma unroll
+    for (int msk = 1; msk < 64; msk <<= 1) { s1 += __shfl_xor(s1, msk); s2 += __shfl_xor(s2, msk); }
     float mean = s1 * (1.f / 128.f);
     float var = s2 * (1.f / 128.f) - mean * mean;
     float inv = rsqrtf(var + 1e-5f);
-    float lv[4] = {v.x, v.y, v.z, v.w};
-    union { unsigned short u[4]; ushort4 v4; } pk;
-#pragma unroll
-    for (int i = 0; i < 4; ++i) {
-      int k = cg5 * 4 + i;
-      pk.u[i] = f2bf((lv[i] - mean) * inv * ln2g[k] + ln2b[k]);
-    }
-    int c8 = cg5 >> 1, hf = cg5 & 1;
-    *(ushort4*)&As[r5 * 128 + ((c8 ^ (r5 & 7)) << 3) + hf * 4] = pk.v4;
+    unsigned u0 = f2bf((x0 - mean) * inv * ln2g[c0] + ln2b[c0]);
+    unsigned u1 = f2bf((x1 - mean) * inv * ln2g[c0 + 1] + ln2b[c0 + 1]);
+    int chunk = lane >> 2, idx2 = (lane & 3) * 2;
+    *(unsigned*)&As[wv * 128 + ((chunk ^ (wv & 7)) << 3) + idx2] = u0 | (u1 << 16);
   }
   __syncthreads();
   {
@@ -754,20 +704,23 @@
       s8v af = *(const s8v*)&As[la * 128 + (((ks * 4 + lb) ^ (la & 7)) << 3)];
 #pragma unroll
       for (int ti = 0; ti < 4; ++ti) {
-        int col = (w * 4 + ti) * 16 + la;
+        int col = (wv * 4 + ti) * 16 + la;
         s8v bf = *(const s8v*)(f1T + (size_t)col * 128 + ks * 32 + lb * 8);
         acc1[ti] = __builtin_amdgcn_mfma_f32_16x16x32_bf16(af, bf, acc1[ti], 0, 0, 0);
       }
     }
 #pragma unroll
     for (int ti = 0; ti < 4; ++ti) {
-      int col = (w * 4 + ti) * 16 + la;
+      int col = (wv * 4 + ti) * 16 + la;
       int chunk = col >> 3, idx = col & 7;
 #pragma unroll
       for (int j = 0; j < 4; ++j) {
         int m = lb * 4 + j;
-        float val = acc1[ti][j] + b1[col];
-        val = 0.5f * val * (1.f + erff(val * 0.70710678118654752f));
+        float val = 0.f;
+        if (m < 8) {
+          val = acc1[ti][j] + b1[col];
+          val = 0.5f * val * (1.f + erff(val * 0.70710678118654752f));
+        }
         Hs[m * 512 + ((chunk ^ (m & 7)) << 3) + idx] = f2bf(val);
       }
     }
@@ -775,7 +728,7 @@
   __syncthreads();
   {
     f4 acc2 = {};
-    int col = w * 16 + la;
+    int col = wv * 16 + la;
 #pragma unroll
     for (int ks = 0; ks < 16; ++ks) {
       s8v af = *(const s8v*)&Hs[la * 512 + (((ks * 4 + lb) ^ (la & 7)) << 3)];
@@ -783,34 +736,33 @@
       acc2 = __builtin_amdgcn_mfma_f32_16x16x32_bf16(af, bf, acc2, 0, 0, 0);
     }
 #pragma unroll
-    for (int j = 0; j < 4; ++j) qtile[lb * 4 + j][col] += acc2[j] + b2[col];
+    for (int j = 0; j < 4; ++j) {
+      int lr = lb * 4 + j;
+      if (lr < 8) qtile[lr][col] += acc2[j] + b2[col];
+    }
   }
   __syncthreads();
   if (CLS) {
-    float ps0 = 0.f, ps1 = 0.f, ps2 = 0.f, ps3 = 0.f;
-#pragma unroll
-    for (int i = 0; i < 4; ++i) {
-      int k = cg5 * 4 + i;
-      float qv = qtile[r5][k];
-      ps0 += qv * cw[k * 4 + 0];
-      ps1 += qv * cw[k * 4 + 1];
-      ps2 += qv * cw[k * 4 + 2];
-      ps3 += qv * cw[k * 4 + 3];
-    }
-#pragma unroll
-    for (int msk = 1; msk < 32; msk <<= 1) {
+    int c0 = lane * 2;
+    float q0 = qtile[wv][c0], q1 = qtile[wv][c0 + 1];
+    float ps0 = q0 * cw[c0 * 4 + 0] + q1 * cw[(c0 + 1) * 4 + 0];
+    float ps1 = q0 * cw[c0 * 4 + 1] + q1 * cw[(c0 + 1) * 4 + 1];
+    float ps2 = q0 * cw[c0 * 4 + 2] + q1 * cw[(c0 + 1) * 4 + 2];
+    float ps3 = q0 * cw[c0 * 4 + 3] + q1 * cw[(c0 + 1) * 4 + 3];
+#pragma unroll
+    for (int msk = 1; msk < 64; msk <<= 1) {
       ps0 += __shfl_xor(ps0, msk);
       ps1 += __shfl_xor(ps1, msk);
       ps2 += __shfl_xor(ps2, msk);
       ps3 += __shfl_xor(ps3, msk);
     }
-    if (cg5 < 4 && row5 < M) {
-      float o = (cg5 == 0) ? ps0 : (cg5 == 1) ? ps1 : (cg5 == 2) ? ps2 : ps3;
-      out[row5 * 4 + cg5] = o + cb[cg5];
+    if (lane < 4) {
+      float o = (lane == 0) ? ps0 : (lane == 1) ? ps1 : (lane == 2) ? ps2 : ps3;
+      out[(m0 + wv) * 4 + lane] = o + cb[lane];
     }
   } else {
-    if (row5 < M)
-      *(float4*)(qb + (size_t)row5 * 128 + cg5 * 4) = *(const float4*)&qtile[r5][cg5 * 4];
+    if (lane < 32)
+      *(float4*)(qb + (size_t)(m0 + wv) * 128 + lane * 4) = *(const float4*)&qtile[wv][lane * 4];
   }
 }
 
@@ -890,8 +842,7 @@
   unsigned short* imgT = (unsigned short*)carve((size_t)BB * NCAM * HWI * 128 * 2);
   unsigned short* vol = (unsigned short*)carve((size_t)BB * NVOX * 128 * 2);
 
-  const int M = BQ;
-  const int GB16 = (M + 15) / 16;
+  const int GB8 = BQ / 8;
 
   mask_k<<<1, 1024, 0, stream>>>(maskp, flag, invden, imc, many);
   tpre_k<<<dim3(2, 2, 165), 256, 0, stream>>>(c_w_w, s_w_w, c_op_w, s_op_w,
@@ -912,27 +863,27 @@
   zero_vol_k<<<1024, 256, 0, stream>>>(vol, winner);
   scatter_winner_k<<<(BQ + 255) / 256, 256, 0, stream>>>(x_idx, y_idx, z_idx, winner);
 
-  cross_mega_k<<<GB16, 512, 0, stream>>>(query, ref_points, maskp, flag, invden, imc, imgT,
-                                         c_ln1_g, c_ln1_b, c_dp_w, c_dp_b, c_a_w, c_a_b,
-                                         WcT, c_op_b, v1buf, v2buf, c_ln2_g, c_ln2_b,
-                                         f1T, c_ff1_b, f2T, c_ff2_b, qb, M);
+  cross_mega_k<<<GB8, 512, 0, stream>>>(query, ref_points, maskp, flag, invden, imc, imgT,
+                                        c_ln1_g, c_ln1_b, c_dp_w, c_dp_b, c_a_w, c_a_b,
+                                        WcT, c_op_b, v1buf, v2buf, c_ln2_g, c_ln2_b,
+                                        f1T, c_ff1_b, f2T, c_ff2_b, qb);
 
   scatter_write_k<<<(BQ * 16 + 255) / 256, 256, 0, stream>>>(x_idx, y_idx, z_idx, winner, qb, vol);
-  self_mega_k<false><<<GB16, 512, 0, stream>>>(qb, ref3d, vol, many,
-                                               s_ln1_g, s_ln1_b, s_dp_w, s_dp_b, s_a_w, s_a_b,
-                                               WcT + (size_t)3 * 16384, s_op_b, csbuf,
-                                               s_ln2_g, s_ln2_b,
-                                               f1T + (size_t)3 * 65536, s_ff1_b,
-                                               f2T + (size_t)3 * 65536, s_ff2_b,
-                                               qb, cls_w, cls_b, out, M);
+  self_mega_k<false><<<GB8, 512, 0, stream>>>(qb, ref3d, vol, many,
+                                              s_ln1_g, s_ln1_b, s_dp_w, s_dp_b, s_a_w, s_a_b,
+                                              WcT + (size_t)3 * 16384, s_op_b, csbuf,
+                                              s_ln2_g, s_ln2_b,
+                                              f1T + (size_t)3 * 65536, s_ff1_b,
+                                              f2T + (size_t)3 * 65536, s_ff2_b,
+                                              qb, cls_w, cls_b, out);
   scatter_write_k<<<(BQ * 16 + 255) / 256, 256, 0, stream>>>(x_idx, y_idx, z_idx, winner, qb, vol);
-  self_mega_k<true><<<GB16, 512, 0, stream>>>(qb, ref3d, vol, many,
-                                              s_ln1_g + 128, s_ln1_b + 128,
-                                              s_dp_w + (size_t)128 * 24, s_dp_b + 24,
-                                              s_a_w + (size_t)128 * 8, s_a_b + 8,
-                                              WcT + (size_t)4 * 16384, s_op_b + 128,
-                                              csbuf + 128, s_ln2_g + 128, s_ln2_b + 128,
-                                              f1T + (size_t)4 * 65536, s_ff1_b + 512,
-                                              f2T + (size_t)4 * 65536, s_ff2_b + 128,
-                                              qb, cls_w, cls_b, out, M);
-}
+  self_mega_k<true><<<GB8, 512, 0, stream>>>(qb, ref3d, vol, many,
+                                             s_ln1_g + 128, s_ln1_b + 128,
+                                             s_dp_w + (size_t)128 * 24, s_dp_b + 24,
+                                             s_a_w + (size_t)128 * 8, s_a_b + 8,
+                                             WcT + (size_t)4 * 16384, s_op_b + 128,
+                                             csbuf + 128, s_ln2_g + 128, s_ln2_b + 128,
+                                             f1T + (size_t)4 * 65536, s_ff1_b + 512,
+                                             f2T + (size_t)4 * 65536, s_ff2_b + 128,
+                                             qb, cls_w, cls_b, out);
+}
```

After: 513.9 us. 1.09x slower.
